# Kernel tuning notes

Hardware: AMD Instinct MI355X
Metric: run time of the kernel (lower is better)

## Reference

```python
import jax, jax.numpy as jnp
import numpy as np

B, TE, TD = 16, 400, 64
E, H = 256, 512
H2 = 2 * H  # 1024
V = 32000


def setup_inputs():
    key = jax.random.key(0)
    k = jax.random.split(key, 16)
    s = 0.05
    return {
        "encoder_inputs": jax.random.randint(k[0], (B, TE), 0, V),
        "decoder_inputs": jax.random.randint(k[1], (B, TD), 0, V),
        "ext_oov_sizes": jax.random.randint(k[2], (B,), 0, 10),
        "enc_idxes_on_ext_voc": jax.random.randint(k[3], (B, TE), 0, V),
        "h0": jnp.zeros((2, B, H), jnp.float32),
        "c0": jnp.zeros((2, B, H), jnp.float32),
        "emb": jax.random.normal(k[4], (V, E)) * 0.1,
        "Wih_f": jax.random.normal(k[5], (4 * H, E)) * s,
        "Whh_f": jax.random.normal(k[6], (4 * H, H)) * s,
        "b_f": jnp.zeros((4 * H,), jnp.float32),
        "Wih_b": jax.random.normal(k[7], (4 * H, E)) * s,
        "Whh_b": jax.random.normal(k[8], (4 * H, H)) * s,
        "b_b": jnp.zeros((4 * H,), jnp.float32),
        "Wih_d": jax.random.normal(k[9], (4 * H2, E + 2 * H2)) * s,
        "Whh_d": jax.random.normal(k[10], (4 * H2, H2)) * s,
        "b_d": jnp.zeros((4 * H2,), jnp.float32),
        "W_ea": jax.random.normal(k[11], (H2, H2)) * 0.006,
        "W_da": jax.random.normal(k[12], (H2, H2)) * 0.006,
        "W_v": jax.random.normal(k[13], (V, 3 * H2)) * s,
        "b_v": jnp.zeros((V,), jnp.float32),
    }


def lstm_cell(x, h, c, Wih, Whh, b):
    z = x @ Wih.T + h @ Whh.T + b
    i, f, g, o = jnp.split(z, 4, axis=-1)
    i, f, o = jax.nn.sigmoid(i), jax.nn.sigmoid(f), jax.nn.sigmoid(o)
    c2 = f * c + i * jnp.tanh(g)
    return o * jnp.tanh(c2), c2


def run_lstm(xs, h0, c0, Wih, Whh, b):
    # xs: [T, B, E]
    def step(carry, x):
        h, c = lstm_cell(x, carry[0], carry[1], Wih, Whh, b)
        return (h, c), h
    (h, c), hs = jax.lax.scan(step, (h0, c0), xs)
    return hs, h, c


def _forward(emb, Wih_f, Whh_f, b_f, Wih_b, Whh_b, b_b, Wih_d, Whh_d, b_d,
             W_ea, W_da, W_v, b_v, h0, c0, encoder_inputs, decoder_inputs):
    xs = emb[encoder_inputs].transpose(1, 0, 2)  # [TE, B, E]
    hs_f, hf, cf = run_lstm(xs, h0[0], c0[0], Wih_f, Whh_f, b_f)
    hs_b, hb, cb = run_lstm(xs[::-1], h0[1], c0[1], Wih_b, Whh_b, b_b)
    enc_out = jnp.concatenate([hs_f, hs_b[::-1]], axis=-1).transpose(1, 0, 2)  # [B, TE, 2H]
    h = jnp.concatenate([hf, hb], axis=-1)  # [B, 2H] (torch reshape of bi-dir last hidden)
    c = jnp.concatenate([cf, cb], axis=-1)
    dec_emb = emb[decoder_inputs].transpose(1, 0, 2)  # [TD, B, E]

    def step(carry, xs_t):
        h, c, accum, buf = carry
        i, emb_t = xs_t
        # intra-temporal encoder attention: exp scores normalized by past accumulation
        scores = jnp.einsum('bd,btd->bt', h @ W_ea, enc_out)  # [B, TE]
        exp_s = jnp.exp(scores)
        denom = jnp.where(i == 0, jnp.ones_like(accum), accum)
        ep = exp_s / denom
        attn = ep / jnp.sum(ep, axis=-1, keepdims=True)
        ctx_e = jnp.einsum('bt,btd->bd', attn, enc_out)
        # intra-decoder attention over previously produced hidden states (masked)
        dsc = jnp.einsum('bd,tbd->bt', h @ W_da, buf)  # [B, TD]
        dsc = jnp.where((jnp.arange(TD) < i)[None, :], dsc, -1e30)
        dw = jnp.where(i == 0, 0.0, jax.nn.softmax(dsc, axis=-1))
        ctx_d = jnp.einsum('bt,tbd->bd', dw, buf)
        x = jnp.concatenate([emb_t, ctx_e, ctx_d], axis=-1)  # [B, E+4H]
        h2, c2 = lstm_cell(x, h, c, Wih_d, Whh_d, b_d)
        buf2 = buf.at[i].set(h2)
        feat = jnp.concatenate([h2, ctx_e, ctx_d], axis=-1)  # [B, 6H]
        logd = jax.nn.log_softmax(feat @ W_v.T + b_v, axis=-1)
        return (h2, c2, accum + exp_s, buf2), logd

    carry0 = (h, c, jnp.zeros((B, TE), h.dtype), jnp.zeros((TD, B, H2), h.dtype))
    (h, c, _, _), logds = jax.lax.scan(step, carry0, (jnp.arange(TD), dec_emb))
    return logds.transpose(1, 0, 2), h[None], c[None]


def reference(encoder_inputs, decoder_inputs, ext_oov_sizes, enc_idxes_on_ext_voc,
              h0, c0, emb, Wih_f, Whh_f, b_f, Wih_b, Whh_b, b_b,
              Wih_d, Whh_d, b_d, W_ea, W_da, W_v, b_v):
    # ext_oov_sizes / enc_idxes_on_ext_voc are unused by forward (as in the torch source)
    return _forward(emb, Wih_f, Whh_f, b_f, Wih_b, Whh_b, b_b, Wih_d, Whh_d, b_d,
                    W_ea, W_da, W_v, b_v, h0, c0, encoder_inputs, decoder_inputs)
```

## Files before the change

### kernel.cpp

```cpp
#include <hip/hip_runtime.h>
#include <math.h>

#define B_  16
#define TE_ 400
#define TD_ 64
#define E_  256
#define H_  512
#define H2_ 1024
#define V_  32000
#define KE_ 768

typedef __attribute__((ext_vector_type(4))) float f32x4;
typedef __attribute__((ext_vector_type(8))) short s16x8;
typedef __attribute__((ext_vector_type(8))) unsigned short u16x8;
typedef __attribute__((ext_vector_type(4))) unsigned short u16x4;

__device__ __forceinline__ float bf2f(unsigned short u){
  union { unsigned int i; float f; } v; v.i = ((unsigned int)u) << 16; return v.f;
}
__device__ __forceinline__ unsigned short f2bf(float f){
  union { float f; unsigned int i; } v; v.f = f;
  return (unsigned short)((v.i + 0x7fffu + ((v.i >> 16) & 1u)) >> 16);
}
__device__ __forceinline__ float sigmoidf_(float x){ return 1.f/(1.f + expf(-x)); }

__device__ __forceinline__ void gl_lds16(const void* gsrc, void* ldst){
  __builtin_amdgcn_global_load_lds(
      (const __attribute__((address_space(1))) unsigned int*)gsrc,
      (__attribute__((address_space(3))) unsigned int*)ldst, 16, 0, 0);
}

__device__ __forceinline__ void bar_arrive(unsigned* obj, unsigned widx){
  __syncthreads();
  if (threadIdx.x == 0){
    __threadfence();
    __hip_atomic_fetch_add(&obj[(widx & 7u)*32], 1u, __ATOMIC_RELAXED, __HIP_MEMORY_SCOPE_AGENT);
  }
}
__device__ __forceinline__ void bar_wait(unsigned* obj, unsigned nwg, unsigned widx, unsigned epoch){
  if (threadIdx.x == 0){
    if (widx == 0){
      for(;;){
        unsigned s = 0;
        #pragma unroll
        for (int k2 = 0; k2 < 8; ++k2)
          s += __hip_atomic_load(&obj[k2*32], __ATOMIC_RELAXED, __HIP_MEMORY_SCOPE_AGENT);
        if (s >= nwg*epoch) break;
      }
      __hip_atomic_store(&obj[256], epoch, __ATOMIC_RELEASE, __HIP_MEMORY_SCOPE_AGENT);
    } else {
      while (__hip_atomic_load(&obj[256], __ATOMIC_RELAXED, __HIP_MEMORY_SCOPE_AGENT) < epoch)
        __builtin_amdgcn_s_sleep(1);
    }
    __threadfence();
  }
  __syncthreads();
}
__device__ __forceinline__ void fast_bar(unsigned* obj, unsigned nwg, unsigned widx, unsigned epoch){
  bar_arrive(obj, widx);
  bar_wait(obj, nwg, widx, epoch);
}

__global__ void k_init(unsigned* bars, float* accum){
  int gid = blockIdx.x*256 + threadIdx.x;
  if (gid < 4096) bars[gid] = 0u;
  if (gid < B_*TE_) accum[gid] = 0.f;
}

__global__ void k_gather(const float* __restrict__ emb, const int* __restrict__ idx,
                         unsigned short* __restrict__ out, int T){
  int wv = threadIdx.x >> 6, l = threadIdx.x & 63;
  int row = blockIdx.x*4 + wv;
  if (row >= T*B_) return;
  int t = row >> 4, b = row & 15;
  int tok = idx[b*T + t];
  float4 v = *(const float4*)(emb + (size_t)tok*E_ + l*4);
  u16x4 o; o[0]=f2bf(v.x); o[1]=f2bf(v.y); o[2]=f2bf(v.z); o[3]=f2bf(v.w);
  *(u16x4*)(out + (size_t)row*E_ + l*4) = o;
}

__global__ void k_prep_enc(const float* __restrict__ Wih_f, const float* __restrict__ Whh_f,
                           const float* __restrict__ Wih_b, const float* __restrict__ Whh_b,
                           unsigned short* __restrict__ Wenc){
  int it = blockIdx.x*256 + threadIdx.x;
  int dir = it / (2048*96); int rem = it % (2048*96);
  int pr = rem / 96; int kc = rem % 96; int k0 = kc*8;
  int g = pr >> 6, r = pr & 63, gate = r >> 4, ul = r & 15;
  int orig = gate*H_ + g*16 + ul;
  const float* Wih = dir ? Wih_b : Wih_f;
  const float* Whh = dir ? Whh_b : Whh_f;
  u16x8 o;
  #pragma unroll
  for (int e = 0; e < 8; ++e){
    int k = k0 + e;
    float v = (k < E_) ? Wih[(size_t)orig*E_ + k] : Whh[(size_t)orig*H_ + (k - E_)];
    o[e] = f2bf(v);
  }
  *(u16x8*)(Wenc + ((size_t)dir*2048 + pr)*KE_ + k0) = o;
}

__global__ void k_prep_whext(const float* __restrict__ Whh_d, const float* __restrict__ W_da,
                             char* __restrict__ WhExt){
  int it = blockIdx.x*256 + threadIdx.x;
  if (it < 524288){
    int g = it >> 13; int rem = it & 8191;
    int kblk = rem >> 10; int rem2 = rem & 1023;
    int row = rem2 >> 4; int k8 = rem2 & 15;
    int gate = row >> 4, ul = row & 15;
    int orig = gate*H2_ + g*16 + ul;
    u16x8 o;
    #pragma unroll
    for (int e = 0; e < 8; ++e)
      o[e] = f2bf(Whh_d[(size_t)orig*H2_ + kblk*128 + k8*8 + e]);
    size_t off = (size_t)g*163840 + (size_t)kblk*20480 + (size_t)(row*256 + ((k8*16) ^ ((row&7)<<4)));
    *(u16x8*)(WhExt + off) = o;
  } else if (it < 655360){
    int qi = it - 524288;
    int g = qi >> 11; int rem = qi & 2047;
    int kblk = rem >> 8; int c2 = rem & 255;
    int wv = c2 >> 6, rr = (c2 >> 2) & 15, c = c2 & 3;
    u16x8 o;
    #pragma unroll
    for (int e = 0; e < 8; ++e)
      o[e] = f2bf(W_da[(size_t)(g*16 + rr)*H2_ + kblk*128 + wv*32 + c*8 + e]);
    size_t off = (size_t)g*163840 + (size_t)kblk*20480 + 16384 + (size_t)(wv*1024 + rr*64 + ((c*16) ^ ((rr&7)<<4)));
    *(u16x8*)(WhExt + off) = o;
  }
}

__global__ void k_prep_ctx(const float* __restrict__ Wih_d, char* __restrict__ CtxW){
  int it = blockIdx.x*256 + threadIdx.x;
  int g = it >> 14; int rem = it & 16383;
  int kblk = rem >> 10; int rem2 = rem & 1023;
  int row = rem2 >> 4; int k8 = rem2 & 15;
  int gate = row >> 4, ul = row & 15;
  int orig = gate*H2_ + g*16 + ul;
  int k = 256 + kblk*128 + k8*8;
  u16x8 o;
  #pragma unroll
  for (int e = 0; e < 8; ++e)
    o[e] = f2bf(Wih_d[(size_t)orig*2304 + k + e]);
  size_t off = (size_t)g*262144 + (size_t)kblk*16384 + (size_t)(row*256 + ((k8*16) ^ ((row&7)<<4)));
  *(u16x8*)(CtxW + off) = o;
}

__global__ void k_prep_wihemb(const float* __restrict__ Wih_d, unsigned short* __restrict__ Wemb){
  int it = blockIdx.x*256 + threadIdx.x;
  int p = it >> 5; int k0 = (it & 31)*8;
  int g = p >> 6, gate = (p >> 4) & 3, ul = p & 15;
  int orig = gate*H2_ + g*16 + ul;
  u16x8 o;
  #pragma unroll
  for (int e = 0; e < 8; ++e)
    o[e] = f2bf(Wih_d[(size_t)orig*2304 + k0 + e]);
  *(u16x8*)(Wemb + (size_t)p*256 + k0) = o;
}

__global__ void __launch_bounds__(256, 2) k_zinit(
    const unsigned short* __restrict__ A,
    const unsigned short* __restrict__ Bw,
    const float* __restrict__ bd,
    float* __restrict__ Cz)
{
  __shared__ unsigned short Ab[128*72];
  __shared__ unsigned short Bt[128*72];
  int p = blockIdx.x;
  int mt = p >> 5, nt = p & 31;
  int m0 = mt*128, n0 = nt*128;
  int tid = threadIdx.x, wvv = tid>>6, l = tid&63;
  int wr = wvv>>1, wc = wvv&1;
  f32x4 zero4 = {0.f,0.f,0.f,0.f};
  f32x4 acc[4][4];
  #pragma unroll
  for (int a=0;a<4;++a){
    #pragma unroll
    for (int b=0;b<4;++b) acc[a][b] = zero4;
  }
  for (int k0 = 0; k0 < 256; k0 += 64){
    #pragma unroll
    for (int qq = 0; qq < 4; ++qq){
      int idx8 = (tid + qq*256)*8;
      int r = idx8 >> 6, k = idx8 & 63;
      *(u16x8*)(Ab + r*72 + k) = *(const u16x8*)(A + (size_t)(m0+r)*256 + k0 + k);
      *(u16x8*)(Bt + r*72 + k) = *(const u16x8*)(Bw + (size_t)(n0+r)*256 + k0 + k);
    }
    __syncthreads();
    #pragma unroll
    for (int ks = 0; ks < 2; ++ks){
      s16x8 af[4], bf[4];
      #pragma unroll
      for (int fi=0;fi<4;++fi)
        af[fi] = *(const s16x8*)(Ab + (wr*64+fi*16+(l&15))*72 + ks*32 + (l>>4)*8);
      #pragma unroll
      for (int fj=0;fj<4;++fj)
        bf[fj] = *(const s16x8*)(Bt + (wc*64+fj*16+(l&15))*72 + ks*32 + (l>>4)*8);
      #pragma unroll
      for (int fi=0;fi<4;++fi){
        #pragma unroll
        for (int fj=0;fj<4;++fj)
          acc[fi][fj] = __builtin_amdgcn_mfma_f32_16x16x32_bf16(af[fi], bf[fj], acc[fi][fj], 0,0,0);
      }
    }
    __syncthreads();
  }
  #pragma unroll
  for (int fj=0;fj<4;++fj){
    int col = n0 + wc*64 + fj*16 + (l&15);
    int orig = ((col>>4)&3)*H2_ + (col>>6)*16 + (col&15);
    float bias = bd[orig];
    #pragma unroll
    for (int fi=0;fi<4;++fi){
      #pragma unroll
      for (int j=0;j<4;++j){
        int row = m0 + wr*64 + fi*16 + (l>>4)*4 + j;
        Cz[(size_t)row*4096 + col] = acc[fi][fj][j] + bias;
      }
    }
  }
}

__global__ void __launch_bounds__(256, 1) k_encoder(
    const unsigned short* __restrict__ xs,
    const unsigned short* __restrict__ Wenc,
    const float* __restrict__ b_f, const float* __restrict__ b_b,
    const float* __restrict__ h0, const float* __restrict__ c0,
    unsigned short* __restrict__ enc_out,
    unsigned short* __restrict__ hbuf,
    float* __restrict__ h0dec, float* __restrict__ c0dec,
    unsigned* __restrict__ bars)
{
  extern __shared__ char smem[];
  unsigned short* Wt = (unsigned short*)smem;
  unsigned short* At = Wt + 64*776;
  float* zl = (float*)(At + 16*776);
  int tid = threadIdx.x;
  int w = blockIdx.x;
  int dir = w >> 5, g = w & 31;
  int wv = tid >> 6, l = tid & 63;
  unsigned* bobj = bars + dir*512;
  {
    const unsigned short* Wsrc = Wenc + ((size_t)dir*2048 + g*64)*KE_;
    int r = tid >> 2, s = tid & 3;
    for (int c = 0; c < 24; ++c)
      *(u16x8*)(Wt + r*776 + s*192 + c*8) = *(const u16x8*)(Wsrc + (size_t)r*KE_ + s*192 + c*8);
  }
  const float* bias = dir ? b_b : b_f;
  int bb = tid >> 4, ul = tid & 15;
  float creg = c0[((size_t)dir*16 + bb)*H_ + g*16 + ul];
  int kchunk = (l >> 4) * 8;
  float bia = bias[wv*H_ + g*16 + (l&15)];
  f32x4 bias4 = { bia, bia, bia, bia };
  f32x4 zero4 = { 0.f, 0.f, 0.f, 0.f };
  {
    int r = tid >> 4, s = tid & 15;
    int tg0 = dir ? (TE_-1) : 0;
    *(u16x8*)(At + r*776 + s*16)     = *(const u16x8*)(xs + ((size_t)tg0*16 + r)*E_ + s*16);
    *(u16x8*)(At + r*776 + s*16 + 8) = *(const u16x8*)(xs + ((size_t)tg0*16 + r)*E_ + s*16 + 8);
    for (int e = 0; e < 32; ++e)
      At[r*776 + 256 + s*32 + e] = f2bf(h0[((size_t)dir*16 + r)*H_ + s*32 + e]);
  }
  __syncthreads();
  for (int t = 0; t < TE_; ++t){
    int tg = dir ? (TE_-1 - t) : t;
    f32x4 acc0 = bias4, acc1 = zero4;
    const unsigned short* brow = Wt + (wv*16 + (l&15))*776 + kchunk;
    const unsigned short* ap   = At + (l&15)*776 + kchunk;
    #pragma unroll
    for (int ks = 0; ks < 24; ++ks){
      s16x8 afr = *(const s16x8*)(ap + ks*32);
      s16x8 bfr = *(const s16x8*)(brow + ks*32);
      if (ks & 1) acc1 = __builtin_amdgcn_mfma_f32_16x16x32_bf16(afr, bfr, acc1, 0, 0, 0);
      else        acc0 = __builtin_amdgcn_mfma_f32_16x16x32_bf16(afr, bfr, acc0, 0, 0, 0);
    }
    f32x4 acc = acc0 + acc1;
    #pragma unroll
    for (int j = 0; j < 4; ++j)
      zl[wv*256 + ((l>>4)*4 + j)*16 + (l&15)] = acc[j];
    __syncthreads();
    float zi = zl[0*256 + bb*16 + ul];
    float zf = zl[1*256 + bb*16 + ul];
    float zg = zl[2*256 + bb*16 + ul];
    float zo = zl[3*256 + bb*16 + ul];
    float iv = sigmoidf_(zi), fv = sigmoidf_(zf), gv = tanhf(zg), ov = sigmoidf_(zo);
    float cc = fv*creg + iv*gv;
    float hh = ov * tanhf(cc);
    creg = cc;
    int u = g*16 + ul;
    unsigned short hb = f2bf(hh);
    hbuf[((size_t)dir*2 + ((t+1)&1))*(16*H_) + bb*H_ + u] = hb;
    enc_out[((size_t)bb*TE_ + tg)*H2_ + dir*H_ + u] = hb;
    if (t == TE_-1){
      h0dec[(size_t)bb*H2_ + dir*H_ + u] = hh;
      c0dec[(size_t)bb*H2_ + dir*H_ + u] = cc;
    }
    bar_arrive(bobj, (unsigned)g);
    if (t+1 < TE_){
      int r = tid >> 4, s = tid & 15;
      int tg2 = dir ? (TE_-2 - t) : (t+1);
      *(u16x8*)(At + r*776 + s*16)     = *(const u16x8*)(xs + ((size_t)tg2*16 + r)*E_ + s*16);
      *(u16x8*)(At + r*776 + s*16 + 8) = *(const u16x8*)(xs + ((size_t)tg2*16 + r)*E_ + s*16 + 8);
    }
    bar_wait(bobj, 32, (unsigned)g, (unsigned)(t+1));
    if (t+1 < TE_){
      int r = tid >> 4, s = tid & 15;
      const unsigned short* hsrc = hbuf + ((size_t)dir*2 + ((t+1)&1))*(16*H_) + r*H_ + s*32;
      for (int c = 0; c < 4; ++c)
        *(u16x8*)(At + r*776 + 256 + s*32 + c*8) = *(const u16x8*)(hsrc + c*8);
    }
    __syncthreads();
  }
}

__global__ void k_dec_init(const float* __restrict__ h0dec, unsigned short* __restrict__ hreg){
  int gid = blockIdx.x*256 + threadIdx.x;
  if (gid < 16384) hreg[gid] = f2bf(h0dec[gid]);
}

__global__ void __launch_bounds__(256, 2) k_penc(
    const unsigned short* __restrict__ enc,
    const float* __restrict__ Wea,
    unsigned short* __restrict__ P)
{
  __shared__ unsigned short Ab[128*72];
  __shared__ unsigned short Bt[128*72];
  int p = blockIdx.x;
  int mt = p >> 3, nt = p & 7;
  int m0 = mt*128, n0 = nt*128;
  int tid = threadIdx.x, wvv = tid>>6, l = tid&63;
  int wr = wvv>>1, wc = wvv&1;
  f32x4 zero4 = {0.f,0.f,0.f,0.f};
  f32x4 acc[4][4];
  #pragma unroll
  for (int a=0;a<4;++a){
    #pragma unroll
    for (int b=0;b<4;++b) acc[a][b] = zero4;
  }
  for (int k0 = 0; k0 < 1024; k0 += 64){
    #pragma unroll
    for (int qq = 0; qq < 4; ++qq){
      int idx8 = (tid + qq*256)*8;
      int r = idx8 >> 6, k = idx8 & 63;
      *(u16x8*)(Ab + r*72 + k) = *(const u16x8*)(enc + (size_t)(m0+r)*1024 + k0 + k);
    }
    #pragma unroll
    for (int qq = 0; qq < 4; ++qq){
      int idx8 = (tid + qq*256)*8;
      int r = idx8 >> 6, k = idx8 & 63;
      const float* src = Wea + (size_t)(n0+r)*1024 + k0 + k;
      float4 v0 = *(const float4*)src;
      float4 v1 = *(const float4*)(src+4);
      u16x8 o;
      o[0]=f2bf(v0.x); o[1]=f2bf(v0.y); o[2]=f2bf(v0.z); o[3]=f2bf(v0.w);
      o[4]=f2bf(v1.x); o[5]=f2bf(v1.y); o[6]=f2bf(v1.z); o[7]=f2bf(v1.w);
      *(u16x8*)(Bt + r*72 + k) = o;
    }
    __syncthreads();
    #pragma unroll
    for (int ks = 0; ks < 2; ++ks){
      s16x8 af[4], bf[4];
      #pragma unroll
      for (int fi=0;fi<4;++fi)
        af[fi] = *(const s16x8*)(Ab + (wr*64+fi*16+(l&15))*72 + ks*32 + (l>>4)*8);
      #pragma unroll
      for (int fj=0;fj<4;++fj)
        bf[fj] = *(const s16x8*)(Bt + (wc*64+fj*16+(l&15))*72 + ks*32 + (l>>4)*8);
      #pragma unroll
      for (int fi=0;fi<4;++fi){
        #pragma unroll
        for (int fj=0;fj<4;++fj)
          acc[fi][fj] = __builtin_amdgcn_mfma_f32_16x16x32_bf16(af[fi], bf[fj], acc[fi][fj], 0,0,0);
      }
    }
    __syncthreads();
  }
  #pragma unroll
  for (int fj=0;fj<4;++fj){
    int col = n0 + wc*64 + fj*16 + (l&15);
    #pragma unroll
    for (int fi=0;fi<4;++fi){
      #pragma unroll
      for (int j=0;j<4;++j){
        int row = m0 + wr*64 + fi*16 + (l>>4)*4 + j;
        P[(size_t)row*1024 + col] = f2bf(acc[fi][fj][j]);
      }
    }
  }
}

__device__ __forceinline__ void issueA(const char* gA, char* Bb, int wv, int l, int kblk, int buf){
  const char* gsrc = gA + (size_t)kblk*20480;
  char* lb = Bb + buf*20480;
  #pragma unroll
  for (int q = 0; q < 4; ++q)
    gl_lds16(gsrc + wv*4096 + q*1024 + (size_t)l*16, lb + wv*4096 + q*1024);
  gl_lds16(gsrc + 16384 + wv*1024 + (size_t)l*16, lb + 16384 + wv*1024);
}
__device__ __forceinline__ void issueC(const char* gC, char* Bb, int wv, int l, int kblk, int buf){
  const char* gsrc = gC + (size_t)kblk*16384;
  char* lb = Bb + buf*20480;
  #pragma unroll
  for (int q = 0; q < 4; ++q)
    gl_lds16(gsrc + wv*4096 + q*1024 + (size_t)l*16, lb + wv*4096 + q*1024);
}

__global__ void __launch_bounds__(256, 1) k_decoder(
  const char* __restrict__ WhExt,
  const char* __restrict__ CtxW,
  const float* __restrict__ zinit,
  const unsigned short* __restrict__ Penc,
  const unsigned short* __restrict__ enc_out,
  const float* __restrict__ c0dec,
  unsigned short* __restrict__ hreg,
  unsigned short* __restrict__ xbuf,
  float* __restrict__ q,
  float* __restrict__ accum,
  float* __restrict__ pctx,
  float* __restrict__ psum,
  unsigned short* __restrict__ bufh,
  unsigned short* __restrict__ Av,
  float* __restrict__ outHC,
  unsigned* __restrict__ bars)
{
  extern __shared__ char smem[];
  int tid = threadIdx.x, w = blockIdx.x;
  int wv = tid >> 6, l = tid & 63;
  unsigned* objA = bars + 1024;
  unsigned* objB = bars + 1536;
  unsigned* objC = bars + 2048;

  unsigned short* Atc = (unsigned short*)smem;
  unsigned short* Ah  = (unsigned short*)smem;
  char*  Bb = smem + 66560;
  float* zl = (float*)(smem + 148480);
  float* zq = (float*)(smem + 152576);
  unsigned short* encL = (unsigned short*)smem;
  float* epL  = (float*)(smem + 102400);
  float* dscL = (float*)(smem + 103424);

  bool isL = (w < 64);
  int eb = 0, ec = 0;
  if (w >= 64){ eb = (w-64) >> 3; ec = (w-64) & 7; }

  if (w >= 64){
    for (int rr = 0; rr < 50; ++rr){
      const unsigned short* src = enc_out + ((size_t)eb*TE_ + ec*50 + rr)*H2_;
      *(u16x4*)(encL + rr*1024 + tid*4) = *(const u16x4*)(src + tid*4);
    }
    __syncthreads();
  }
  float creg = 0.f;
  int bb = tid >> 4, ul = tid & 15;
  const char* gA = (const char*)WhExt + (size_t)w*163840;
  const char* gC = (const char*)CtxW + (size_t)w*262144;

  f32x4 acc0, acc1;

  for (int i = 0; i < TD_; ++i){
    if (isL){
      issueA(gA, Bb, wv, l, 0, 0);
      issueA(gA, Bb, wv, l, 1, 1);
      {
        int r = tid >> 4, s = tid & 15;
        const unsigned short* hsrc = hreg + (i&1)*16384 + r*H2_ + s*64;
        for (int c = 0; c < 8; ++c)
          *(u16x8*)(Ah + r*1032 + s*64 + c*8) = *(const u16x8*)(hsrc + c*8);
      }
      __syncthreads();
      {
        const float* zsrc = zinit + ((size_t)i*16 + (l>>4)*4)*4096 + w*64 + wv*16 + (l&15);
        f32x4 a; a[0]=zsrc[0]; a[1]=zsrc[4096]; a[2]=zsrc[8192]; a[3]=zsrc[12288];
        acc0 = a;
        f32x4 z4 = {0.f,0.f,0.f,0.f};
        acc1 = z4;
      }
      f32x4 accq = {0.f,0.f,0.f,0.f};
      int swz = ((l&7)<<4);
      for (int kblk = 0; kblk < 8; ++kblk){
        int buf = kblk % 3;
        if (kblk + 2 < 8) issueA(gA, Bb, wv, l, kblk+2, (kblk+2)%3);
        if (kblk < 6)       asm volatile("s_waitcnt vmcnt(10)" ::: "memory");
        else if (kblk == 6) asm volatile("s_waitcnt vmcnt(5)" ::: "memory");
        else                asm volatile("s_waitcnt vmcnt(0)" ::: "memory");
        const unsigned short* ap = Ah + (l&15)*1032 + kblk*128 + (l>>4)*8;
        const char* Bz = Bb + buf*20480 + wv*4096;
        #pragma unroll
        for (int ks = 0; ks < 4; ++ks){
          int k8 = ks*4 + (l>>4);
          s16x8 afr = *(const s16x8*)(ap + ks*32);
          s16x8 bfr = *(const s16x8*)(Bz + (l&15)*256 + ((k8*16) ^ swz));
          if (ks & 1) acc1 = __builtin_amdgcn_mfma_f32_16x16x32_bf16(afr, bfr, acc1, 0,0,0);
          else        acc0 = __builtin_amdgcn_mfma_f32_16x16x32_bf16(afr, bfr, acc0, 0,0,0);
        }
        {
          s16x8 afq = *(const s16x8*)(Ah + (l&15)*1032 + kblk*128 + wv*32 + (l>>4)*8);
          s16x8 bfq = *(const s16x8*)(Bb + buf*20480 + 16384 + wv*1024 + (l&15)*64 + ((((l>>4)*16)) ^ swz));
          accq = __builtin_amdgcn_mfma_f32_16x16x32_bf16(afq, bfq, accq, 0,0,0);
        }
      }
      #pragma unroll
      for (int j = 0; j < 4; ++j)
        zq[wv*256 + ((l>>4)*4+j)*16 + (l&15)] = accq[j];
      __syncthreads();
      float qv = zq[0*256 + bb*16 + ul] + zq[1*256 + bb*16 + ul]
               + zq[2*256 + bb*16 + ul] + zq[3*256 + bb*16 + ul];
      q[(size_t)bb*H2_ + w*16 + ul] = qv;
    } else {
      const unsigned short* hb_ = hreg + (i&1)*16384 + eb*H2_ + l*16;
      u16x8 hv0 = *(const u16x8*)hb_;
      u16x8 hv1 = *(const u16x8*)(hb_ + 8);
      float hf[16];
      #pragma unroll
      for (int c = 0; c < 8; ++c){ hf[c] = bf2f(hv0[c]); hf[8+c] = bf2f(hv1[c]); }
      for (int rr = wv; rr < 50; rr += 4){
        const unsigned short* pr = Penc + ((size_t)(eb*TE_ + ec*50 + rr))*H2_ + l*16;
        u16x8 p0 = *(const u16x8*)pr;
        u16x8 p1 = *(const u16x8*)(pr + 8);
        float sc = 0.f;
        #pragma unroll
        for (int c = 0; c < 8; ++c) sc += hf[c]*bf2f(p0[c]);
        #pragma unroll
        for (int c = 0; c < 8; ++c) sc += hf[8+c]*bf2f(p1[c]);
        #pragma unroll
        for (int o = 1; o < 64; o <<= 1) sc += __shfl_xor(sc, o);
        if (l == 0){
          int t = ec*50 + rr;
          float es = expf(sc);
          float aold = accum[eb*TE_ + t];
          float denom = (i == 0) ? 1.f : aold;
          accum[eb*TE_ + t] = aold + es;
          epL[rr] = es / denom;
        }
      }
      __syncthreads();
      float tot = 0.f;
      for (int rr = 0; rr < 50; ++rr) tot += epL[rr];
      float a0=0.f,a1=0.f,a2=0.f,a3=0.f;
      for (int rr = 0; rr < 50; ++rr){
        float wgt = epL[rr];
        u16x4 ev = *(const u16x4*)(encL + rr*1024 + tid*4);
        a0 += wgt*bf2f(ev[0]); a1 += wgt*bf2f(ev[1]); a2 += wgt*bf2f(ev[2]); a3 += wgt*bf2f(ev[3]);
      }
      int slot = w - 64;
      float4 o4; o4.x=a0; o4.y=a1; o4.z=a2; o4.w=a3;
      *(float4*)(pctx + (size_t)slot*1024 + tid*4) = o4;
      if (tid == 0) psum[slot] = tot;
      __syncthreads();
    }
    fast_bar(objA, 192, (unsigned)w, (unsigned)(i+1));

    if (isL){
      #pragma unroll
      for (int j = 0; j < 4; ++j)
        issueC(gC, Bb, wv, l, j, j);
    } else if (w < 96){
      int b = (w-64) >> 1, half = w & 1;
      int col = half*512 + tid*2;
      if (i == 0){
        *(unsigned*)(xbuf + (size_t)b*2048 + 1024 + col) = 0u;
        *(unsigned*)(Av + ((size_t)b*TD_ + i)*3072 + 2048 + col) = 0u;
      } else {
        const float* qp = q + (size_t)b*H2_ + l*16;
        float4 q0 = *(const float4*)(qp);
        float4 q1 = *(const float4*)(qp+4);
        float4 q2 = *(const float4*)(qp+8);
        float4 q3 = *(const float4*)(qp+12);
        for (int tp = wv; tp < i; tp += 4){
          const unsigned short* br = bufh + ((size_t)tp*16 + b)*H2_ + l*16;
          u16x8 e0 = *(const u16x8*)(br);
          u16x8 e1 = *(const u16x8*)(br + 8);
          float sc = q0.x*bf2f(e0[0]) + q0.y*bf2f(e0[1]) + q0.z*bf2f(e0[2]) + q0.w*bf2f(e0[3])
                   + q1.x*bf2f(e0[4]) + q1.y*bf2f(e0[5]) + q1.z*bf2f(e0[6]) + q1.w*bf2f(e0[7])
                   + q2.x*bf2f(e1[0]) + q2.y*bf2f(e1[1]) + q2.z*bf2f(e1[2]) + q2.w*bf2f(e1[3])
                   + q3.x*bf2f(e1[4]) + q3.y*bf2f(e1[5]) + q3.z*bf2f(e1[6]) + q3.w*bf2f(e1[7]);
          #pragma unroll
          for (int o = 1; o < 64; o <<= 1) sc += __shfl_xor(sc, o);
          if (l == 0) dscL[tp] = sc;
        }
        __syncthreads();
        float scv = (l < i) ? dscL[l] : -1e30f;
        float m = scv;
        #pragma unroll
        for (int o = 1; o < 64; o <<= 1) m = fmaxf(m, __shfl_xor(m, o));
        float e = (l < i) ? expf(scv - m) : 0.f;
        float ssum = e;
        #pragma unroll
        for (int o = 1; o < 64; o <<= 1) ssum += __shfl_xor(ssum, o);
        float wgt = e / ssum;
        float c0_ = 0.f, c1_ = 0.f;
        for (int tp = 0; tp < i; ++tp){
          float wt = __shfl(wgt, tp);
          unsigned hv = *(const unsigned*)(bufh + ((size_t)tp*16 + b)*H2_ + col);
          c0_ += wt*bf2f((unsigned short)hv);
          c1_ += wt*bf2f((unsigned short)(hv>>16));
        }
        unsigned o2 = (unsigned)f2bf(c0_) | ((unsigned)f2bf(c1_) << 16);
        *(unsigned*)(xbuf + (size_t)b*2048 + 1024 + col) = o2;
        *(unsigned*)(Av + ((size_t)b*TD_ + i)*3072 + 2048 + col) = o2;
      }
    } else if (w < 112){
      int b = w - 96;
      float sx=0.f, sy=0.f, sz=0.f, sw=0.f, pst=0.f;
      for (int c = 0; c < 8; ++c){
        float4 v = *(const float4*)(pctx + (size_t)(b*8+c)*1024 + tid*4);
        sx += v.x; sy += v.y; sz += v.z; sw += v.w;
        pst += psum[b*8+c];
      }
      float inv = 1.f/pst;
      u16x4 o; o[0]=f2bf(sx*inv); o[1]=f2bf(sy*inv); o[2]=f2bf(sz*inv); o[3]=f2bf(sw*inv);
      *(u16x4*)(xbuf + (size_t)b*2048 + tid*4) = o;
      *(u16x4*)(Av + ((size_t)b*TD_ + i)*3072 + 1024 + tid*4) = o;
    }
    fast_bar(objB, 192, (unsigned)w, (unsigned)(i+1));

    if (isL){
      {
        int r = tid >> 4, s = tid & 15;
        for (int c = 0; c < 16; ++c)
          *(u16x8*)(Atc + r*2056 + s*128 + c*8) = *(const u16x8*)(xbuf + (size_t)r*2048 + s*128 + c*8);
      }
      __syncthreads();
      int swz = ((l&7)<<4);
      for (int kblk = 0; kblk < 16; ++kblk){
        int buf = kblk & 3;
        if (kblk >= 4 && kblk <= 12) asm volatile("s_waitcnt vmcnt(12)" ::: "memory");
        else if (kblk == 13)         asm volatile("s_waitcnt vmcnt(8)" ::: "memory");
        else if (kblk == 14)         asm volatile("s_waitcnt vmcnt(4)" ::: "memory");
        else if (kblk == 15)         asm volatile("s_waitcnt vmcnt(0)" ::: "memory");
        const unsigned short* ap = Atc + (l&15)*2056 + kblk*128 + (l>>4)*8;
        const char* Bz = Bb + buf*20480 + wv*4096;
        #pragma unroll
        for (int ks = 0; ks < 4; ++ks){
          int k8 = ks*4 + (l>>4);
          s16x8 afr = *(const s16x8*)(ap + ks*32);
          s16x8 bfr = *(const s16x8*)(Bz + (l&15)*256 + ((k8*16) ^ swz));
          if (ks & 1) acc1 = __builtin_amdgcn_mfma_f32_16x16x32_bf16(afr, bfr, acc1, 0,0,0);
          else        acc0 = __builtin_amdgcn_mfma_f32_16x16x32_bf16(afr, bfr, acc0, 0,0,0);
        }
        if (kblk + 4 < 16) issueC(gC, Bb, wv, l, kblk+4, buf);
      }
      f32x4 acc = acc0 + acc1;
      #pragma unroll
      for (int j = 0; j < 4; ++j)
        zl[wv*256 + ((l>>4)*4+j)*16 + (l&15)] = acc[j];
      __syncthreads();
      float zi = zl[0*256 + bb*16 + ul];
      float zf = zl[1*256 + bb*16 + ul];
      float zg = zl[2*256 + bb*16 + ul];
      float zo = zl[3*256 + bb*16 + ul];
      if (i == 0) creg = c0dec[(size_t)bb*H2_ + w*16 + ul];
      float iv = sigmoidf_(zi), fv = sigmoidf_(zf), gv = tanhf(zg), ov = sigmoidf_(zo);
      float cc = fv*creg + iv*gv;
      float hh = ov*tanhf(cc);
      creg = cc;
      int u = w*16 + ul;
      unsigned short hb2 = f2bf(hh);
      hreg[((i+1)&1)*16384 + (size_t)bb*H2_ + u] = hb2;
      Av[((size_t)bb*TD_ + i)*3072 + u] = hb2;
      bufh[((size_t)i*16 + bb)*H2_ + u] = hb2;
      if (i == TD_-1){
        outHC[(size_t)bb*H2_ + u] = hh;
        outHC[16384 + (size_t)bb*H2_ + u] = cc;
      }
    }
    fast_bar(objC, 192, (unsigned)w, (unsigned)(i+1));
  }
}

__global__ void __launch_bounds__(256, 2) k_vocab_gemm(
    const unsigned short* __restrict__ Av,
    const float* __restrict__ Wv,
    const float* __restrict__ bv,
    float* __restrict__ out)
{
  __shared__ unsigned short Ab[128*72];
  __shared__ unsigned short Bt[128*72];
  int p = blockIdx.x;
  int mt = (p>>3)&7, nt = (p&7) + 8*(p>>6);
  if (nt >= 250) return;
  int m0 = mt*128, n0 = nt*128;
  int tid = threadIdx.x, wvv = tid>>6, l = tid&63;
  int wr = wvv>>1, wc = wvv&1;
  f32x4 zero4 = {0.f,0.f,0.f,0.f};
  f32x4 acc[4][4];
  #pragma unroll
  for (int a=0;a<4;++a){
    #pragma unroll
    for (int b=0;b<4;++b) acc[a][b] = zero4;
  }
  for (int k0 = 0; k0 < 3072; k0 += 64){
    #pragma unroll
    for (int qq = 0; qq < 4; ++qq){
      int idx8 = (tid + qq*256)*8;
      int r = idx8 >> 6, k = idx8 & 63;
      *(u16x8*)(Ab + r*72 + k) = *(const u16x8*)(Av + (size_t)(m0+r)*3072 + k0 + k);
    }
    #pragma unroll
    for (int qq = 0; qq < 4; ++qq){
      int idx8 = (tid + qq*256)*8;
      int r = idx8 >> 6, k = idx8 & 63;
      const float* src = Wv + (size_t)(n0+r)*3072 + k0 + k;
      float4 v0 = *(const float4*)src;
      float4 v1 = *(const float4*)(src+4);
      u16x8 o;
      o[0]=f2bf(v0.x); o[1]=f2bf(v0.y); o[2]=f2bf(v0.z); o[3]=f2bf(v0.w);
      o[4]=f2bf(v1.x); o[5]=f2bf(v1.y); o[6]=f2bf(v1.z); o[7]=f2bf(v1.w);
      *(u16x8*)(Bt + r*72 + k) = o;
    }
    __syncthreads();
    #pragma unroll
    for (int ks = 0; ks < 2; ++ks){
      s16x8 af[4], bf[4];
      #pragma unroll
      for (int fi=0;fi<4;++fi)
        af[fi] = *(const s16x8*)(Ab + (wr*64+fi*16+(l&15))*72 + ks*32 + (l>>4)*8);
      #pragma unroll
      for (int fj=0;fj<4;++fj)
        bf[fj] = *(const s16x8*)(Bt + (wc*64+fj*16+(l&15))*72 + ks*32 + (l>>4)*8);
      #pragma unroll
      for (int fi=0;fi<4;++fi){
        #pragma unroll
        for (int fj=0;fj<4;++fj)
          acc[fi][fj] = __builtin_amdgcn_mfma_f32_16x16x32_bf16(af[fi], bf[fj], acc[fi][fj], 0,0,0);
      }
    }
    __syncthreads();
  }
  #pragma unroll
  for (int fj=0;fj<4;++fj){
    int col = n0 + wc*64 + fj*16 + (l&15);
    float bias = bv[col];
    #pragma unroll
    for (int fi=0;fi<4;++fi){
      #pragma unroll
      for (int j=0;j<4;++j){
        int row = m0 + wr*64 + fi*16 + (l>>4)*4 + j;
        out[(size_t)row*V_ + col] = acc[fi][fj][j] + bias;
      }
    }
  }
}

__global__ void k_logsoftmax(float* __restrict__ out){
  int row = blockIdx.x;
  float* x = out + (size_t)row*V_;
  int tid = threadIdx.x;
  __shared__ float red[64];
  float m = -1e30f;
  for (int c = tid; c < V_; c += 256) m = fmaxf(m, x[c]);
  #pragma unroll
  for (int o=1;o<64;o<<=1) m = fmaxf(m, __shfl_xor(m,o));
  if ((tid&63)==0) red[tid>>6] = m;
  __syncthreads();
  m = fmaxf(fmaxf(red[0],red[1]), fmaxf(red[2],red[3]));
  float s = 0.f;
  for (int c = tid; c < V_; c += 256) s += expf(x[c]-m);
  #pragma unroll
  for (int o=1;o<64;o<<=1) s += __shfl_xor(s,o);
  if ((tid&63)==0) red[8 + (tid>>6)] = s;
  __syncthreads();
  s = red[8]+red[9]+red[10]+red[11];
  float lse = m + logf(s);
  for (int c = tid; c < V_; c += 256) x[c] = x[c] - lse;
}

extern "C" void kernel_launch(void* const* d_in, const int* in_sizes, int n_in,
                              void* d_out, int out_size, void* d_ws, size_t ws_size,
                              hipStream_t stream){
  (void)in_sizes; (void)n_in; (void)out_size; (void)ws_size;
  const int*   enc_in = (const int*)d_in[0];
  const int*   dec_in = (const int*)d_in[1];
  const float* h0   = (const float*)d_in[4];
  const float* c0   = (const float*)d_in[5];
  const float* emb  = (const float*)d_in[6];
  const float* Wih_f= (const float*)d_in[7];
  const float* Whh_f= (const float*)d_in[8];
  const float* b_f  = (const float*)d_in[9];
  const float* Wih_b= (const float*)d_in[10];
  const float* Whh_b= (const float*)d_in[11];
  const float* b_b  = (const float*)d_in[12];
  const float* Wih_d= (const float*)d_in[13];
  const float* Whh_d= (const float*)d_in[14];
  const float* b_d  = (const float*)d_in[15];
  const float* W_ea = (const float*)d_in[16];
  const float* W_da = (const float*)d_in[17];
  const float* W_v  = (const float*)d_in[18];
  const float* b_v  = (const float*)d_in[19];
  float* out = (float*)d_out;
  char* ws = (char*)d_ws;

  size_t o_bars   = 0;
  size_t o_accum  = 16384;
  size_t o_q      = o_accum + 25600;
  size_t o_xs     = o_q + 65536;
  size_t o_decemb = o_xs + (size_t)6400*256*2;
  size_t o_Wenc   = o_decemb + (size_t)1024*256*2;
  size_t o_WhExt  = o_Wenc + (size_t)2*2048*768*2;
  size_t o_CtxW   = o_WhExt + (size_t)64*163840;
  size_t o_Wemb   = o_CtxW + (size_t)64*262144;
  size_t o_zinit  = o_Wemb + (size_t)4096*256*2;
  size_t o_enc    = o_zinit + (size_t)1024*4096*4;
  size_t o_Penc   = o_enc + (size_t)16*400*1024*2;
  size_t o_hbuf   = o_Penc + (size_t)16*400*1024*2;
  size_t o_h0dec  = o_hbuf + (size_t)2*2*16*512*2;
  size_t o_c0dec  = o_h0dec + (size_t)16*1024*4;
  size_t o_hreg   = o_c0dec + (size_t)16*1024*4;
  size_t o_xbuf   = o_hreg + (size_t)2*16*1024*2;
  size_t o_pctx   = o_xbuf + (size_t)16*2048*2;
  size_t o_psum   = o_pctx + (size_t)128*1024*4;
  size_t o_bufh   = o_psum + 512;
  size_t o_Av     = o_bufh + (size_t)64*16*1024*2;

  unsigned* bars        = (unsigned*)(ws + o_bars);
  float* accum          = (float*)(ws + o_accum);
  float* q              = (float*)(ws + o_q);
  unsigned short* xs    = (unsigned short*)(ws + o_xs);
  unsigned short* decemb= (unsigned short*)(ws + o_decemb);
  unsigned short* Wenc  = (unsigned short*)(ws + o_Wenc);
  char* WhExt           = ws + o_WhExt;
  char* CtxW            = ws + o_CtxW;
  unsigned short* Wemb  = (unsigned short*)(ws + o_Wemb);
  float* zinit          = (float*)(ws + o_zinit);
  unsigned short* encO  = (unsigned short*)(ws + o_enc);
  unsigned short* Penc  = (unsigned short*)(ws + o_Penc);
  unsigned short* hbuf  = (unsigned short*)(ws + o_hbuf);
  float* h0dec          = (float*)(ws + o_h0dec);
  float* c0dec          = (float*)(ws + o_c0dec);
  unsigned short* hreg  = (unsigned short*)(ws + o_hreg);
  unsigned short* xbuf  = (unsigned short*)(ws + o_xbuf);
  float* pctx           = (float*)(ws + o_pctx);
  float* psum           = (float*)(ws + o_psum);
  unsigned short* bufh  = (unsigned short*)(ws + o_bufh);
  unsigned short* Av    = (unsigned short*)(ws + o_Av);

  hipFuncSetAttribute((const void*)k_encoder, hipFuncAttributeMaxDynamicSharedMemorySize, 131072);
  hipFuncSetAttribute((const void*)k_decoder, hipFuncAttributeMaxDynamicSharedMemorySize, 157696);

  k_init<<<26, 256, 0, stream>>>(bars, accum);
  k_gather<<<1600, 256, 0, stream>>>(emb, enc_in, xs, TE_);
  k_gather<<<256, 256, 0, stream>>>(emb, dec_in, decemb, TD_);
  k_prep_enc<<<1536, 256, 0, stream>>>(Wih_f, Whh_f, Wih_b, Whh_b, Wenc);
  k_prep_whext<<<2560, 256, 0, stream>>>(Whh_d, W_da, WhExt);
  k_prep_ctx<<<4096, 256, 0, stream>>>(Wih_d, CtxW);
  k_prep_wihemb<<<512, 256, 0, stream>>>(Wih_d, Wemb);
  k_zinit<<<256, 256, 0, stream>>>(decemb, Wemb, b_d, zinit);
  k_encoder<<<64, 256, 128512, stream>>>(xs, Wenc, b_f, b_b, h0, c0, encO, hbuf, h0dec, c0dec, bars);
  k_penc<<<400, 256, 0, stream>>>(encO, W_ea, Penc);
  k_dec_init<<<64, 256, 0, stream>>>(h0dec, hreg);
  k_decoder<<<192, 256, 156672, stream>>>(WhExt, CtxW, zinit, Penc, encO, c0dec,
                                          hreg, xbuf, q, accum, pctx, psum, bufh, Av,
                                          out + (size_t)32768000, bars);
  k_vocab_gemm<<<2048, 256, 0, stream>>>(Av, W_v, b_v, out);
  k_logsoftmax<<<1024, 256, 0, stream>>>(out);
}
```

Baseline: 6.342 ms.

## Hoist encoder input projection, overlap weight prep with encoder, restructure decoder sync

A new batched MFMA GEMM computes the encoder input projections (x·Wih + bias) for all timesteps ahead of time, so the recurrent encoder loop only multiplies by Whh (K=512 instead of 768). Decoder weight preparation moves into extra workgroups of the encoder launch so it runs alongside the sequential recurrence. The global barrier is replaced with per-timestep counters and backoff polling. The decoder is reorganised into specialised roles (matrix, encoder attention, decoder attention) that synchronise through separate barriers and accumulate context with atomics. These changes cost extra workspace for the zx buffer, add atomic traffic, and make correctness depend on more complex synchronisation.

```diff
diff --git a/kernel.cpp b/kernel.cpp
--- a/kernel.cpp
+++ b/kernel.cpp
@@ -8,7 +8,6 @@
 #define H_  512
 #define H2_ 1024
 #define V_  32000
-#define KE_ 768
 
 typedef __attribute__((ext_vector_type(4))) float f32x4;
 typedef __attribute__((ext_vector_type(8))) short s16x8;
@@ -30,41 +29,30 @@
       (__attribute__((address_space(3))) unsigned int*)ldst, 16, 0, 0);
 }
 
-__device__ __forceinline__ void bar_arrive(unsigned* obj, unsigned widx){
-  __syncthreads();
-  if (threadIdx.x == 0){
-    __threadfence();
-    __hip_atomic_fetch_add(&obj[(widx & 7u)*32], 1u, __ATOMIC_RELAXED, __HIP_MEMORY_SCOPE_AGENT);
-  }
-}
-__device__ __forceinline__ void bar_wait(unsigned* obj, unsigned nwg, unsigned widx, unsigned epoch){
-  if (threadIdx.x == 0){
-    if (widx == 0){
-      for(;;){
-        unsigned s = 0;
-        #pragma unroll
-        for (int k2 = 0; k2 < 8; ++k2)
-          s += __hip_atomic_load(&obj[k2*32], __ATOMIC_RELAXED, __HIP_MEMORY_SCOPE_AGENT);
-        if (s >= nwg*epoch) break;
-      }
-      __hip_atomic_store(&obj[256], epoch, __ATOMIC_RELEASE, __HIP_MEMORY_SCOPE_AGENT);
-    } else {
-      while (__hip_atomic_load(&obj[256], __ATOMIC_RELAXED, __HIP_MEMORY_SCOPE_AGENT) < epoch)
-        __builtin_amdgcn_s_sleep(1);
-    }
-    __threadfence();
-  }
-  __syncthreads();
-}
-__device__ __forceinline__ void fast_bar(unsigned* obj, unsigned nwg, unsigned widx, unsigned epoch){
-  bar_arrive(obj, widx);
-  bar_wait(obj, nwg, widx, epoch);
-}
-
-__global__ void k_init(unsigned* bars, float* accum){
+__device__ __forceinline__ void arrive8(unsigned* inst){
+  __threadfence();
+  __hip_atomic_fetch_add(inst + (blockIdx.x & 7u)*16, 1u, __ATOMIC_RELAXED, __HIP_MEMORY_SCOPE_AGENT);
+}
+__device__ __forceinline__ void poll8(unsigned* inst, unsigned target){
+  int it = 0;
+  for(;;){
+    unsigned s = 0;
+    #pragma unroll
+    for (int k = 0; k < 8; ++k)
+      s += __hip_atomic_load(inst + k*16, __ATOMIC_RELAXED, __HIP_MEMORY_SCOPE_AGENT);
+    if (s >= target) break;
+    if (it < 6) __builtin_amdgcn_s_sleep(1);
+    else if (it < 24) __builtin_amdgcn_s_sleep(4);
+    else __builtin_amdgcn_s_sleep(16);
+    ++it;
+  }
+}
+
+__global__ void k_init(unsigned* bars, float* ctxn, float* psumT){
   int gid = blockIdx.x*256 + threadIdx.x;
-  if (gid < 4096) bars[gid] = 0u;
-  if (gid < B_*TE_) accum[gid] = 0.f;
+  if (gid < 81920) bars[gid] = 0u;
+  if (gid < 32768) ctxn[gid] = 0.f;
+  if (gid < 32) psumT[gid] = 0.f;
 }
 
 __global__ void k_gather(const float* __restrict__ emb, const int* __restrict__ idx,
@@ -96,12 +84,12 @@
     float v = (k < E_) ? Wih[(size_t)orig*E_ + k] : Whh[(size_t)orig*H_ + (k - E_)];
     o[e] = f2bf(v);
   }
-  *(u16x8*)(Wenc + ((size_t)dir*2048 + pr)*KE_ + k0) = o;
-}
-
-__global__ void k_prep_whext(const float* __restrict__ Whh_d, const float* __restrict__ W_da,
-                             char* __restrict__ WhExt){
-  int it = blockIdx.x*256 + threadIdx.x;
+  *(u16x8*)(Wenc + ((size_t)dir*2048 + pr)*768 + k0) = o;
+}
+
+__device__ __forceinline__ void prep_whext_item(int it, const float* __restrict__ Whh_d,
+                                                const float* __restrict__ W_da,
+                                                char* __restrict__ WhExt){
   if (it < 524288){
     int g = it >> 13; int rem = it & 8191;
     int kblk = rem >> 10; int rem2 = rem & 1023;
@@ -118,18 +106,20 @@
     int qi = it - 524288;
     int g = qi >> 11; int rem = qi & 2047;
     int kblk = rem >> 8; int c2 = rem & 255;
-    int wv = c2 >> 6, rr = (c2 >> 2) & 15, c = c2 & 3;
+    int wvv = c2 >> 6, rr = (c2 >> 2) & 15, c = c2 & 3;
+    int row = g*16 + rr;
     u16x8 o;
     #pragma unroll
     for (int e = 0; e < 8; ++e)
-      o[e] = f2bf(W_da[(size_t)(g*16 + rr)*H2_ + kblk*128 + wv*32 + c*8 + e]);
-    size_t off = (size_t)g*163840 + (size_t)kblk*20480 + 16384 + (size_t)(wv*1024 + rr*64 + ((c*16) ^ ((rr&7)<<4)));
+      o[e] = f2bf(W_da[(size_t)row*H2_ + kblk*128 + wvv*32 + c*8 + e]);
+    size_t off = (size_t)g*163840 + (size_t)kblk*20480 + 16384
+               + (size_t)(wvv*1024 + rr*64 + ((c*16) ^ ((rr&3)<<4)));
     *(u16x8*)(WhExt + off) = o;
   }
 }
 
-__global__ void k_prep_ctx(const float* __restrict__ Wih_d, char* __restrict__ CtxW){
-  int it = blockIdx.x*256 + threadIdx.x;
+__device__ __forceinline__ void prep_ctx_item(int it, const float* __restrict__ Wih_d,
+                                              char* __restrict__ CtxW){
   int g = it >> 14; int rem = it & 16383;
   int kblk = rem >> 10; int rem2 = rem & 1023;
   int row = rem2 >> 4; int k8 = rem2 & 15;
@@ -219,54 +209,194 @@
   }
 }
 
-__global__ void __launch_bounds__(256, 1) k_encoder(
+__global__ void __launch_bounds__(256, 2) k_zx(
     const unsigned short* __restrict__ xs,
     const unsigned short* __restrict__ Wenc,
     const float* __restrict__ b_f, const float* __restrict__ b_b,
+    unsigned short* __restrict__ zx)
+{
+  __shared__ unsigned short Ab[128*72];
+  __shared__ unsigned short Bt[128*72];
+  int pblk = blockIdx.x;
+  int dir = pblk / 800; int rem = pblk % 800;
+  int mt = rem >> 4, nt = rem & 15;
+  int m0 = mt*128, n0 = nt*128;
+  int tid = threadIdx.x, wvv = tid>>6, l = tid&63;
+  int wr = wvv>>1, wc = wvv&1;
+  f32x4 zero4 = {0.f,0.f,0.f,0.f};
+  f32x4 acc[4][4];
+  #pragma unroll
+  for (int a=0;a<4;++a){
+    #pragma unroll
+    for (int b=0;b<4;++b) acc[a][b] = zero4;
+  }
+  for (int k0 = 0; k0 < 256; k0 += 64){
+    #pragma unroll
+    for (int qq = 0; qq < 4; ++qq){
+      int idx8 = (tid + qq*256)*8;
+      int r = idx8 >> 6, k = idx8 & 63;
+      *(u16x8*)(Ab + r*72 + k) = *(const u16x8*)(xs + (size_t)(m0+r)*256 + k0 + k);
+      *(u16x8*)(Bt + r*72 + k) = *(const u16x8*)(Wenc + ((size_t)dir*2048 + n0+r)*768 + k0 + k);
+    }
+    __syncthreads();
+    #pragma unroll
+    for (int ks = 0; ks < 2; ++ks){
+      s16x8 af[4], bf[4];
+      #pragma unroll
+      for (int fi=0;fi<4;++fi)
+        af[fi] = *(const s16x8*)(Ab + (wr*64+fi*16+(l&15))*72 + ks*32 + (l>>4)*8);
+      #pragma unroll
+      for (int fj=0;fj<4;++fj)
+        bf[fj] = *(const s16x8*)(Bt + (wc*64+fj*16+(l&15))*72 + ks*32 + (l>>4)*8);
+      #pragma unroll
+      for (int fi=0;fi<4;++fi){
+        #pragma unroll
+        for (int fj=0;fj<4;++fj)
+          acc[fi][fj] = __builtin_amdgcn_mfma_f32_16x16x32_bf16(af[fi], bf[fj], acc[fi][fj], 0,0,0);
+      }
+    }
+    __syncthreads();
+  }
+  const float* bsrc = dir ? b_b : b_f;
+  #pragma unroll
+  for (int fj=0;fj<4;++fj){
+    int col = n0 + wc*64 + fj*16 + (l&15);
+    float bias = bsrc[((col>>4)&3)*512 + (col>>6)*16 + (col&15)];
+    #pragma unroll
+    for (int fi=0;fi<4;++fi){
+      #pragma unroll
+      for (int j=0;j<4;++j){
+        int row = m0 + wr*64 + fi*16 + (l>>4)*4 + j;
+        zx[((size_t)dir*6400 + row)*2048 + col] = f2bf(acc[fi][fj][j] + bias);
+      }
+    }
+  }
+}
+
+__global__ void __launch_bounds__(256, 2) k_penc(
+    const unsigned short* __restrict__ enc,
+    const float* __restrict__ Wea,
+    unsigned short* __restrict__ P)
+{
+  __shared__ unsigned short Ab[128*72];
+  __shared__ unsigned short Bt[128*72];
+  int p = blockIdx.x;
+  int mt = p >> 3, nt = p & 7;
+  int m0 = mt*128, n0 = nt*128;
+  int tid = threadIdx.x, wvv = tid>>6, l = tid&63;
+  int wr = wvv>>1, wc = wvv&1;
+  f32x4 zero4 = {0.f,0.f,0.f,0.f};
+  f32x4 acc[4][4];
+  #pragma unroll
+  for (int a=0;a<4;++a){
+    #pragma unroll
+    for (int b=0;b<4;++b) acc[a][b] = zero4;
+  }
+  for (int k0 = 0; k0 < 1024; k0 += 64){
+    #pragma unroll
+    for (int qq = 0; qq < 4; ++qq){
+      int idx8 = (tid + qq*256)*8;
+      int r = idx8 >> 6, k = idx8 & 63;
+      *(u16x8*)(Ab + r*72 + k) = *(const u16x8*)(enc + (size_t)(m0+r)*1024 + k0 + k);
+    }
+    #pragma unroll
+    for (int qq = 0; qq < 4; ++qq){
+      int idx8 = (tid + qq*256)*8;
+      int r = idx8 >> 6, k = idx8 & 63;
+      const float* src = Wea + (size_t)(n0+r)*1024 + k0 + k;
+      float4 v0 = *(const float4*)src;
+      float4 v1 = *(const float4*)(src+4);
+      u16x8 o;
+      o[0]=f2bf(v0.x); o[1]=f2bf(v0.y); o[2]=f2bf(v0.z); o[3]=f2bf(v0.w);
+      o[4]=f2bf(v1.x); o[5]=f2bf(v1.y); o[6]=f2bf(v1.z); o[7]=f2bf(v1.w);
+      *(u16x8*)(Bt + r*72 + k) = o;
+    }
+    __syncthreads();
+    #pragma unroll
+    for (int ks = 0; ks < 2; ++ks){
+      s16x8 af[4], bf[4];
+      #pragma unroll
+      for (int fi=0;fi<4;++fi)
+        af[fi] = *(const s16x8*)(Ab + (wr*64+fi*16+(l&15))*72 + ks*32 + (l>>4)*8);
+      #pragma unroll
+      for (int fj=0;fj<4;++fj)
+        bf[fj] = *(const s16x8*)(Bt + (wc*64+fj*16+(l&15))*72 + ks*32 + (l>>4)*8);
+      #pragma unroll
+      for (int fi=0;fi<4;++fi){
+        #pragma unroll
+        for (int fj=0;fj<4;++fj)
+          acc[fi][fj] = __builtin_amdgcn_mfma_f32_16x16x32_bf16(af[fi], bf[fj], acc[fi][fj], 0,0,0);
+      }
+    }
+    __syncthreads();
+  }
+  #pragma unroll
+  for (int fj=0;fj<4;++fj){
+    int col = n0 + wc*64 + fj*16 + (l&15);
+    #pragma unroll
+    for (int fi=0;fi<4;++fi){
+      #pragma unroll
+      for (int j=0;j<4;++j){
+        int row = m0 + wr*64 + fi*16 + (l>>4)*4 + j;
+        P[(size_t)row*1024 + col] = f2bf(acc[fi][fj][j]);
+      }
+    }
+  }
+}
+
+__global__ void __launch_bounds__(256, 1) k_encoder(
+    const unsigned short* __restrict__ zx,
+    const unsigned short* __restrict__ Wenc,
     const float* __restrict__ h0, const float* __restrict__ c0,
     unsigned short* __restrict__ enc_out,
     unsigned short* __restrict__ hbuf,
     float* __restrict__ h0dec, float* __restrict__ c0dec,
-    unsigned* __restrict__ bars)
+    unsigned* __restrict__ bars,
+    const float* __restrict__ Whh_d, const float* __restrict__ W_da,
+    const float* __restrict__ Wih_d,
+    char* __restrict__ WhExt, char* __restrict__ CtxW)
 {
   extern __shared__ char smem[];
-  unsigned short* Wt = (unsigned short*)smem;
-  unsigned short* At = Wt + 64*776;
-  float* zl = (float*)(At + 16*776);
   int tid = threadIdx.x;
   int w = blockIdx.x;
+  if (w >= 64){
+    int base = (w - 64)*256 + tid;
+    for (int it = base; it < 655360; it += 36864) prep_whext_item(it, Whh_d, W_da, WhExt);
+    for (int it = base; it < 1048576; it += 36864) prep_ctx_item(it, Wih_d, CtxW);
+    return;
+  }
+  unsigned short* Wt = (unsigned short*)smem;
+  unsigned short* At = Wt + 64*520;
+  float* zl = (float*)(At + 16*520);
   int dir = w >> 5, g = w & 31;
   int wv = tid >> 6, l = tid & 63;
-  unsigned* bobj = bars + dir*512;
   {
-    const unsigned short* Wsrc = Wenc + ((size_t)dir*2048 + g*64)*KE_;
+    const unsigned short* Wsrc = Wenc + ((size_t)dir*2048 + g*64)*768 + 256;
     int r = tid >> 2, s = tid & 3;
-    for (int c = 0; c < 24; ++c)
-      *(u16x8*)(Wt + r*776 + s*192 + c*8) = *(const u16x8*)(Wsrc + (size_t)r*KE_ + s*192 + c*8);
-  }
-  const float* bias = dir ? b_b : b_f;
+    for (int c = 0; c < 16; ++c)
+      *(u16x8*)(Wt + r*520 + s*128 + c*8) = *(const u16x8*)(Wsrc + (size_t)r*768 + s*128 + c*8);
+  }
   int bb = tid >> 4, ul = tid & 15;
   float creg = c0[((size_t)dir*16 + bb)*H_ + g*16 + ul];
   int kchunk = (l >> 4) * 8;
-  float bia = bias[wv*H_ + g*16 + (l&15)];
-  f32x4 bias4 = { bia, bia, bia, bia };
   f32x4 zero4 = { 0.f, 0.f, 0.f, 0.f };
   {
     int r = tid >> 4, s = tid & 15;
-    int tg0 = dir ? (TE_-1) : 0;
-    *(u16x8*)(At + r*776 + s*16)     = *(const u16x8*)(xs + ((size_t)tg0*16 + r)*E_ + s*16);
-    *(u16x8*)(At + r*776 + s*16 + 8) = *(const u16x8*)(xs + ((size_t)tg0*16 + r)*E_ + s*16 + 8);
     for (int e = 0; e < 32; ++e)
-      At[r*776 + 256 + s*32 + e] = f2bf(h0[((size_t)dir*16 + r)*H_ + s*32 + e]);
-  }
+      At[r*520 + s*32 + e] = f2bf(h0[((size_t)dir*16 + r)*H_ + s*32 + e]);
+  }
+  int tg0 = dir ? (TE_-1) : 0;
+  const unsigned short* zrow = zx + ((size_t)dir*6400 + (size_t)tg0*16 + (l>>4)*4)*2048 + g*64 + wv*16 + (l&15);
+  f32x4 a0cur;
+  a0cur[0]=bf2f(zrow[0]); a0cur[1]=bf2f(zrow[2048]); a0cur[2]=bf2f(zrow[4096]); a0cur[3]=bf2f(zrow[6144]);
   __syncthreads();
   for (int t = 0; t < TE_; ++t){
     int tg = dir ? (TE_-1 - t) : t;
-    f32x4 acc0 = bias4, acc1 = zero4;
-    const unsigned short* brow = Wt + (wv*16 + (l&15))*776 + kchunk;
-    const unsigned short* ap   = At + (l&15)*776 + kchunk;
-    #pragma unroll
-    for (int ks = 0; ks < 24; ++ks){
+    f32x4 acc0 = a0cur, acc1 = zero4;
+    const unsigned short* brow = Wt + (wv*16 + (l&15))*520 + kchunk;
+    const unsigned short* ap   = At + (l&15)*520 + kchunk;
+    #pragma unroll
+    for (int ks = 0; ks < 16; ++ks){
       s16x8 afr = *(const s16x8*)(ap + ks*32);
       s16x8 bfr = *(const s16x8*)(brow + ks*32);
       if (ks & 1) acc1 = __builtin_amdgcn_mfma_f32_16x16x32_bf16(afr, bfr, acc1, 0, 0, 0);
@@ -293,19 +423,37 @@
       h0dec[(size_t)bb*H2_ + dir*H_ + u] = hh;
       c0dec[(size_t)bb*H2_ + dir*H_ + u] = cc;
     }
-    bar_arrive(bobj, (unsigned)g);
+    unsigned* cnt = bars + (size_t)(dir*400 + t)*64;
+    __syncthreads();
+    if (tid == 0){
+      __threadfence();
+      __hip_atomic_fetch_add(cnt + (g&3)*16, 1u, __ATOMIC_RELAXED, __HIP_MEMORY_SCOPE_AGENT);
+    }
     if (t+1 < TE_){
-      int r = tid >> 4, s = tid & 15;
       int tg2 = dir ? (TE_-2 - t) : (t+1);
-      *(u16x8*)(At + r*776 + s*16)     = *(const u16x8*)(xs + ((size_t)tg2*16 + r)*E_ + s*16);
-      *(u16x8*)(At + r*776 + s*16 + 8) = *(const u16x8*)(xs + ((size_t)tg2*16 + r)*E_ + s*16 + 8);
-    }
-    bar_wait(bobj, 32, (unsigned)g, (unsigned)(t+1));
+      const unsigned short* zr2 = zx + ((size_t)dir*6400 + (size_t)tg2*16 + (l>>4)*4)*2048 + g*64 + wv*16 + (l&15);
+      a0cur[0]=bf2f(zr2[0]); a0cur[1]=bf2f(zr2[2048]); a0cur[2]=bf2f(zr2[4096]); a0cur[3]=bf2f(zr2[6144]);
+    }
+    if (tid == 0){
+      int it = 0;
+      for(;;){
+        unsigned s_ = 0;
+        #pragma unroll
+        for (int k2 = 0; k2 < 4; ++k2)
+          s_ += __hip_atomic_load(cnt + k2*16, __ATOMIC_RELAXED, __HIP_MEMORY_SCOPE_AGENT);
+        if (s_ >= 32) break;
+        if (it < 6) __builtin_amdgcn_s_sleep(1);
+        else __builtin_amdgcn_s_sleep(4);
+        ++it;
+      }
+      __threadfence();
+    }
+    __syncthreads();
     if (t+1 < TE_){
       int r = tid >> 4, s = tid & 15;
       const unsigned short* hsrc = hbuf + ((size_t)dir*2 + ((t+1)&1))*(16*H_) + r*H_ + s*32;
       for (int c = 0; c < 4; ++c)
-        *(u16x8*)(At + r*776 + 256 + s*32 + c*8) = *(const u16x8*)(hsrc + c*8);
+        *(u16x8*)(At + r*520 + s*32 + c*8) = *(const u16x8*)(hsrc + c*8);
     }
     __syncthreads();
   }
@@ -316,88 +464,17 @@
   if (gid < 16384) hreg[gid] = f2bf(h0dec[gid]);
 }
 
-__global__ void __launch_bounds__(256, 2) k_penc(
-    const unsigned short* __restrict__ enc,
-    const float* __restrict__ Wea,
-    unsigned short* __restrict__ P)
-{
-  __shared__ unsigned short Ab[128*72];
-  __shared__ unsigned short Bt[128*72];
-  int p = blockIdx.x;
-  int mt = p >> 3, nt = p & 7;
-  int m0 = mt*128, n0 = nt*128;
-  int tid = threadIdx.x, wvv = tid>>6, l = tid&63;
-  int wr = wvv>>1, wc = wvv&1;
-  f32x4 zero4 = {0.f,0.f,0.f,0.f};
-  f32x4 acc[4][4];
-  #pragma unroll
-  for (int a=0;a<4;++a){
-    #pragma unroll
-    for (int b=0;b<4;++b) acc[a][b] = zero4;
-  }
-  for (int k0 = 0; k0 < 1024; k0 += 64){
-    #pragma unroll
-    for (int qq = 0; qq < 4; ++qq){
-      int idx8 = (tid + qq*256)*8;
-      int r = idx8 >> 6, k = idx8 & 63;
-      *(u16x8*)(Ab + r*72 + k) = *(const u16x8*)(enc + (size_t)(m0+r)*1024 + k0 + k);
-    }
-    #pragma unroll
-    for (int qq = 0; qq < 4; ++qq){
-      int idx8 = (tid + qq*256)*8;
-      int r = idx8 >> 6, k = idx8 & 63;
-      const float* src = Wea + (size_t)(n0+r)*1024 + k0 + k;
-      float4 v0 = *(const float4*)src;
-      float4 v1 = *(const float4*)(src+4);
-      u16x8 o;
-      o[0]=f2bf(v0.x); o[1]=f2bf(v0.y); o[2]=f2bf(v0.z); o[3]=f2bf(v0.w);
-      o[4]=f2bf(v1.x); o[5]=f2bf(v1.y); o[6]=f2bf(v1.z); o[7]=f2bf(v1.w);
-      *(u16x8*)(Bt + r*72 + k) = o;
-    }
-    __syncthreads();
-    #pragma unroll
-    for (int ks = 0; ks < 2; ++ks){
-      s16x8 af[4], bf[4];
-      #pragma unroll
-      for (int fi=0;fi<4;++fi)
-        af[fi] = *(const s16x8*)(Ab + (wr*64+fi*16+(l&15))*72 + ks*32 + (l>>4)*8);
-      #pragma unroll
-      for (int fj=0;fj<4;++fj)
-        bf[fj] = *(const s16x8*)(Bt + (wc*64+fj*16+(l&15))*72 + ks*32 + (l>>4)*8);
-      #pragma unroll
-      for (int fi=0;fi<4;++fi){
-        #pragma unroll
-        for (int fj=0;fj<4;++fj)
-          acc[fi][fj] = __builtin_amdgcn_mfma_f32_16x16x32_bf16(af[fi], bf[fj], acc[fi][fj], 0,0,0);
-      }
-    }
-    __syncthreads();
-  }
-  #pragma unroll
-  for (int fj=0;fj<4;++fj){
-    int col = n0 + wc*64 + fj*16 + (l&15);
-    #pragma unroll
-    for (int fi=0;fi<4;++fi){
-      #pragma unroll
-      for (int j=0;j<4;++j){
-        int row = m0 + wr*64 + fi*16 + (l>>4)*4 + j;
-        P[(size_t)row*1024 + col] = f2bf(acc[fi][fj][j]);
-      }
-    }
-  }
-}
-
-__device__ __forceinline__ void issueA(const char* gA, char* Bb, int wv, int l, int kblk, int buf){
+__device__ __forceinline__ void issueA(const char* gA, char* BbA, int wv, int l, int kblk, int buf){
   const char* gsrc = gA + (size_t)kblk*20480;
-  char* lb = Bb + buf*20480;
+  char* lb = BbA + buf*20480;
   #pragma unroll
   for (int q = 0; q < 4; ++q)
     gl_lds16(gsrc + wv*4096 + q*1024 + (size_t)l*16, lb + wv*4096 + q*1024);
   gl_lds16(gsrc + 16384 + wv*1024 + (size_t)l*16, lb + 16384 + wv*1024);
 }
-__device__ __forceinline__ void issueC(const char* gC, char* Bb, int wv, int l, int kblk, int buf){
+__device__ __forceinline__ void issueC(const char* gC, char* BbC, int wv, int l, int kblk, int buf){
   const char* gsrc = gC + (size_t)kblk*16384;
-  char* lb = Bb + buf*20480;
+  char* lb = BbC + buf*16384;
   #pragma unroll
   for (int q = 0; q < 4; ++q)
     gl_lds16(gsrc + wv*4096 + q*1024 + (size_t)l*16, lb + wv*4096 + q*1024);
@@ -412,10 +489,9 @@
   const float* __restrict__ c0dec,
   unsigned short* __restrict__ hreg,
   unsigned short* __restrict__ xbuf,
-  float* __restrict__ q,
-  float* __restrict__ accum,
-  float* __restrict__ pctx,
-  float* __restrict__ psum,
+  float* __restrict__ ctxn,
+  float* __restrict__ psumT,
+  unsigned short* __restrict__ vbuf,
   unsigned short* __restrict__ bufh,
   unsigned short* __restrict__ Av,
   float* __restrict__ outHC,
@@ -424,65 +500,72 @@
   extern __shared__ char smem[];
   int tid = threadIdx.x, w = blockIdx.x;
   int wv = tid >> 6, l = tid & 63;
-  unsigned* objA = bars + 1024;
-  unsigned* objB = bars + 1536;
-  unsigned* objC = bars + 2048;
+  unsigned* dbase = bars + 51200;
 
   unsigned short* Atc = (unsigned short*)smem;
   unsigned short* Ah  = (unsigned short*)smem;
-  char*  Bb = smem + 66560;
-  float* zl = (float*)(smem + 148480);
-  float* zq = (float*)(smem + 152576);
+  char* BbA = smem + 66560;
+  char* BbC = smem + 128000;
+  float* zq = (float*)(smem + 66560);
+  float* zl = (float*)(smem + 128000);
   unsigned short* encL = (unsigned short*)smem;
-  float* epL  = (float*)(smem + 102400);
-  float* dscL = (float*)(smem + 103424);
-
-  bool isL = (w < 64);
+  float* epL  = (float*)(smem + 103424);
+  float* accL = (float*)(smem + 103680);
+  float* dscL = (float*)smem;
+
+  bool isZ = (w < 64);
+  bool isE = (w >= 64 && w < 192);
   int eb = 0, ec = 0;
-  if (w >= 64){ eb = (w-64) >> 3; ec = (w-64) & 7; }
-
-  if (w >= 64){
+  if (isE){ eb = (w-64) >> 3; ec = (w-64) & 7; }
+  int db = w - 192;
+
+  if (isE){
     for (int rr = 0; rr < 50; ++rr){
       const unsigned short* src = enc_out + ((size_t)eb*TE_ + ec*50 + rr)*H2_;
-      *(u16x4*)(encL + rr*1024 + tid*4) = *(const u16x4*)(src + tid*4);
-    }
+      *(u16x4*)(encL + rr*1032 + tid*4) = *(const u16x4*)(src + tid*4);
+    }
+    if (tid < 50) accL[tid] = 0.f;
     __syncthreads();
   }
   float creg = 0.f;
   int bb = tid >> 4, ul = tid & 15;
-  const char* gA = (const char*)WhExt + (size_t)w*163840;
-  const char* gC = (const char*)CtxW + (size_t)w*262144;
-
+  const char* gA = WhExt + (size_t)w*163840;
+  const char* gC = CtxW + (size_t)w*262144;
   f32x4 acc0, acc1;
 
   for (int i = 0; i < TD_; ++i){
-    if (isL){
-      issueA(gA, Bb, wv, l, 0, 0);
-      issueA(gA, Bb, wv, l, 1, 1);
+    int p = i & 1;
+    unsigned* barM = dbase + (size_t)(i*3+0)*128;
+    unsigned* barA = dbase + (size_t)(i*3+1)*128;
+    unsigned* barB = dbase + (size_t)(i*3+2)*128;
+
+    if (isZ){
+      ctxn[(p^1)*16384 + w*256 + tid] = 0.f;
+      if (w == 0 && tid < 16) psumT[(p^1)*16 + tid] = 0.f;
+      const float* zsrc = zinit + ((size_t)i*16 + (l>>4)*4)*4096 + w*64 + wv*16 + (l&15);
+      f32x4 a0i; a0i[0]=zsrc[0]; a0i[1]=zsrc[4096]; a0i[2]=zsrc[8192]; a0i[3]=zsrc[12288];
+      issueA(gA, BbA, wv, l, 0, 0);
+      issueA(gA, BbA, wv, l, 1, 1);
       {
         int r = tid >> 4, s = tid & 15;
-        const unsigned short* hsrc = hreg + (i&1)*16384 + r*H2_ + s*64;
+        const unsigned short* hsrc = hreg + p*16384 + r*H2_ + s*64;
         for (int c = 0; c < 8; ++c)
           *(u16x8*)(Ah + r*1032 + s*64 + c*8) = *(const u16x8*)(hsrc + c*8);
       }
       __syncthreads();
-      {
-        const float* zsrc = zinit + ((size_t)i*16 + (l>>4)*4)*4096 + w*64 + wv*16 + (l&15);
-        f32x4 a; a[0]=zsrc[0]; a[1]=zsrc[4096]; a[2]=zsrc[8192]; a[3]=zsrc[12288];
-        acc0 = a;
-        f32x4 z4 = {0.f,0.f,0.f,0.f};
-        acc1 = z4;
-      }
-      f32x4 accq = {0.f,0.f,0.f,0.f};
+      acc0 = a0i;
+      f32x4 z4 = {0.f,0.f,0.f,0.f};
+      acc1 = z4;
+      f32x4 accv = z4;
       int swz = ((l&7)<<4);
       for (int kblk = 0; kblk < 8; ++kblk){
         int buf = kblk % 3;
-        if (kblk + 2 < 8) issueA(gA, Bb, wv, l, kblk+2, (kblk+2)%3);
+        if (kblk + 2 < 8) issueA(gA, BbA, wv, l, kblk+2, (kblk+2)%3);
         if (kblk < 6)       asm volatile("s_waitcnt vmcnt(10)" ::: "memory");
         else if (kblk == 6) asm volatile("s_waitcnt vmcnt(5)" ::: "memory");
         else                asm volatile("s_waitcnt vmcnt(0)" ::: "memory");
         const unsigned short* ap = Ah + (l&15)*1032 + kblk*128 + (l>>4)*8;
-        const char* Bz = Bb + buf*20480 + wv*4096;
+        const char* Bz = BbA + buf*20480 + wv*4096;
         #pragma unroll
         for (int ks = 0; ks < 4; ++ks){
           int k8 = ks*4 + (l>>4);
@@ -491,143 +574,51 @@
           if (ks & 1) acc1 = __builtin_amdgcn_mfma_f32_16x16x32_bf16(afr, bfr, acc1, 0,0,0);
           else        acc0 = __builtin_amdgcn_mfma_f32_16x16x32_bf16(afr, bfr, acc0, 0,0,0);
         }
-        {
-          s16x8 afq = *(const s16x8*)(Ah + (l&15)*1032 + kblk*128 + wv*32 + (l>>4)*8);
-          s16x8 bfq = *(const s16x8*)(Bb + buf*20480 + 16384 + wv*1024 + (l&15)*64 + ((((l>>4)*16)) ^ swz));
-          accq = __builtin_amdgcn_mfma_f32_16x16x32_bf16(afq, bfq, accq, 0,0,0);
-        }
-      }
+        s16x8 afq = *(const s16x8*)(Ah + (l&15)*1032 + kblk*128 + wv*32 + (l>>4)*8);
+        s16x8 bfv = *(const s16x8*)(BbA + buf*20480 + 16384 + wv*1024 + (l&15)*64 + ((((l>>4)*16)) ^ ((l&3)<<4)));
+        accv = __builtin_amdgcn_mfma_f32_16x16x32_bf16(afq, bfv, accv, 0,0,0);
+      }
+      __syncthreads();
       #pragma unroll
       for (int j = 0; j < 4; ++j)
-        zq[wv*256 + ((l>>4)*4+j)*16 + (l&15)] = accq[j];
-      __syncthreads();
-      float qv = zq[0*256 + bb*16 + ul] + zq[1*256 + bb*16 + ul]
-               + zq[2*256 + bb*16 + ul] + zq[3*256 + bb*16 + ul];
-      q[(size_t)bb*H2_ + w*16 + ul] = qv;
-    } else {
-      const unsigned short* hb_ = hreg + (i&1)*16384 + eb*H2_ + l*16;
-      u16x8 hv0 = *(const u16x8*)hb_;
-      u16x8 hv1 = *(const u16x8*)(hb_ + 8);
-      float hf[16];
-      #pragma unroll
-      for (int c = 0; c < 8; ++c){ hf[c] = bf2f(hv0[c]); hf[8+c] = bf2f(hv1[c]); }
-      for (int rr = wv; rr < 50; rr += 4){
-        const unsigned short* pr = Penc + ((size_t)(eb*TE_ + ec*50 + rr))*H2_ + l*16;
-        u16x8 p0 = *(const u16x8*)pr;
-        u16x8 p1 = *(const u16x8*)(pr + 8);
-        float sc = 0.f;
-        #pragma unroll
-        for (int c = 0; c < 8; ++c) sc += hf[c]*bf2f(p0[c]);
-        #pragma unroll
-        for (int c = 0; c < 8; ++c) sc += hf[8+c]*bf2f(p1[c]);
-        #pragma unroll
-        for (int o = 1; o < 64; o <<= 1) sc += __shfl_xor(sc, o);
-        if (l == 0){
-          int t = ec*50 + rr;
-          float es = expf(sc);
-          float aold = accum[eb*TE_ + t];
-          float denom = (i == 0) ? 1.f : aold;
-          accum[eb*TE_ + t] = aold + es;
-          epL[rr] = es / denom;
-        }
-      }
-      __syncthreads();
-      float tot = 0.f;
-      for (int rr = 0; rr < 50; ++rr) tot += epL[rr];
-      float a0=0.f,a1=0.f,a2=0.f,a3=0.f;
-      for (int rr = 0; rr < 50; ++rr){
-        float wgt = epL[rr];
-        u16x4 ev = *(const u16x4*)(encL + rr*1024 + tid*4);
-        a0 += wgt*bf2f(ev[0]); a1 += wgt*bf2f(ev[1]); a2 += wgt*bf2f(ev[2]); a3 += wgt*bf2f(ev[3]);
-      }
-      int slot = w - 64;
-      float4 o4; o4.x=a0; o4.y=a1; o4.z=a2; o4.w=a3;
-      *(float4*)(pctx + (size_t)slot*1024 + tid*4) = o4;
-      if (tid == 0) psum[slot] = tot;
-      __syncthreads();
-    }
-    fast_bar(objA, 192, (unsigned)w, (unsigned)(i+1));
-
-    if (isL){
-      #pragma unroll
-      for (int j = 0; j < 4; ++j)
-        issueC(gC, Bb, wv, l, j, j);
-    } else if (w < 96){
-      int b = (w-64) >> 1, half = w & 1;
-      int col = half*512 + tid*2;
-      if (i == 0){
-        *(unsigned*)(xbuf + (size_t)b*2048 + 1024 + col) = 0u;
-        *(unsigned*)(Av + ((size_t)b*TD_ + i)*3072 + 2048 + col) = 0u;
-      } else {
-        const float* qp = q + (size_t)b*H2_ + l*16;
-        float4 q0 = *(const float4*)(qp);
-        float4 q1 = *(const float4*)(qp+4);
-        float4 q2 = *(const float4*)(qp+8);
-        float4 q3 = *(const float4*)(qp+12);
-        for (int tp = wv; tp < i; tp += 4){
-          const unsigned short* br = bufh + ((size_t)tp*16 + b)*H2_ + l*16;
-          u16x8 e0 = *(const u16x8*)(br);
-          u16x8 e1 = *(const u16x8*)(br + 8);
-          float sc = q0.x*bf2f(e0[0]) + q0.y*bf2f(e0[1]) + q0.z*bf2f(e0[2]) + q0.w*bf2f(e0[3])
-                   + q1.x*bf2f(e0[4]) + q1.y*bf2f(e0[5]) + q1.z*bf2f(e0[6]) + q1.w*bf2f(e0[7])
-                   + q2.x*bf2f(e1[0]) + q2.y*bf2f(e1[1]) + q2.z*bf2f(e1[2]) + q2.w*bf2f(e1[3])
-                   + q3.x*bf2f(e1[4]) + q3.y*bf2f(e1[5]) + q3.z*bf2f(e1[6]) + q3.w*bf2f(e1[7]);
-          #pragma unroll
-          for (int o = 1; o < 64; o <<= 1) sc += __shfl_xor(sc, o);
-          if (l == 0) dscL[tp] = sc;
-        }
-        __syncthreads();
-        float scv = (l < i) ? dscL[l] : -1e30f;
-        float m = scv;
-        #pragma unroll
-        for (int o = 1; o < 64; o <<= 1) m = fmaxf(m, __shfl_xor(m, o));
-        float e = (l < i) ? expf(scv - m) : 0.f;
-        float ssum = e;
-        #pragma unroll
-        for (int o = 1; o < 64; o <<= 1) ssum += __shfl_xor(ssum, o);
-        float wgt = e / ssum;
-        float c0_ = 0.f, c1_ = 0.f;
-        for (int tp = 0; tp < i; ++tp){
-          float wt = __shfl(wgt, tp);
-          unsigned hv = *(const unsigned*)(bufh + ((size_t)tp*16 + b)*H2_ + col);
-          c0_ += wt*bf2f((unsigned short)hv);
-          c1_ += wt*bf2f((unsigned short)(hv>>16));
-        }
-        unsigned o2 = (unsigned)f2bf(c0_) | ((unsigned)f2bf(c1_) << 16);
-        *(unsigned*)(xbuf + (size_t)b*2048 + 1024 + col) = o2;
-        *(unsigned*)(Av + ((size_t)b*TD_ + i)*3072 + 2048 + col) = o2;
-      }
-    } else if (w < 112){
-      int b = w - 96;
-      float sx=0.f, sy=0.f, sz=0.f, sw=0.f, pst=0.f;
-      for (int c = 0; c < 8; ++c){
-        float4 v = *(const float4*)(pctx + (size_t)(b*8+c)*1024 + tid*4);
-        sx += v.x; sy += v.y; sz += v.z; sw += v.w;
-        pst += psum[b*8+c];
-      }
-      float inv = 1.f/pst;
-      u16x4 o; o[0]=f2bf(sx*inv); o[1]=f2bf(sy*inv); o[2]=f2bf(sz*inv); o[3]=f2bf(sw*inv);
-      *(u16x4*)(xbuf + (size_t)b*2048 + tid*4) = o;
-      *(u16x4*)(Av + ((size_t)b*TD_ + i)*3072 + 1024 + tid*4) = o;
-    }
-    fast_bar(objB, 192, (unsigned)w, (unsigned)(i+1));
-
-    if (isL){
+        zq[wv*256 + ((l>>4)*4+j)*16 + (l&15)] = accv[j];
+      __syncthreads();
+      if (i > 0){
+        float vv = zq[0*256+bb*16+ul] + zq[1*256+bb*16+ul] + zq[2*256+bb*16+ul] + zq[3*256+bb*16+ul];
+        vbuf[((size_t)(i-1)*16 + bb)*H2_ + w*16 + ul] = f2bf(vv);
+      }
+      __syncthreads();
+      if (tid == 0) arrive8(barM);
+      issueC(gC, BbC, wv, l, 0, 0);
+      issueC(gC, BbC, wv, l, 1, 1);
+      if (tid == 0){ poll8(barA, 144); __threadfence(); }
+      __syncthreads();
       {
         int r = tid >> 4, s = tid & 15;
-        for (int c = 0; c < 16; ++c)
-          *(u16x8*)(Atc + r*2056 + s*128 + c*8) = *(const u16x8*)(xbuf + (size_t)r*2048 + s*128 + c*8);
-      }
-      __syncthreads();
-      int swz = ((l&7)<<4);
-      for (int kblk = 0; kblk < 16; ++kblk){
-        int buf = kblk & 3;
-        if (kblk >= 4 && kblk <= 12) asm volatile("s_waitcnt vmcnt(12)" ::: "memory");
-        else if (kblk == 13)         asm volatile("s_waitcnt vmcnt(8)" ::: "memory");
-        else if (kblk == 14)         asm volatile("s_waitcnt vmcnt(4)" ::: "memory");
-        else if (kblk == 15)         asm volatile("s_waitcnt vmcnt(0)" ::: "memory");
-        const unsigned short* ap = Atc + (l&15)*2056 + kblk*128 + (l>>4)*8;
-        const char* Bz = Bb + buf*20480 + wv*4096;
+        float inv = 1.f / psumT[p*16 + r];
+        const float* cn = ctxn + p*16384 + (size_t)r*1024 + s*64;
+        for (int c8 = 0; c8 < 8; ++c8){
+          float4 v0 = *(const float4*)(cn + c8*8);
+          float4 v1 = *(const float4*)(cn + c8*8 + 4);
+          u16x8 o;
+          o[0]=f2bf(v0.x*inv); o[1]=f2bf(v0.y*inv); o[2]=f2bf(v0.z*inv); o[3]=f2bf(v0.w*inv);
+          o[4]=f2bf(v1.x*inv); o[5]=f2bf(v1.y*inv); o[6]=f2bf(v1.z*inv); o[7]=f2bf(v1.w*inv);
+          *(u16x8*)(Atc + r*2056 + s*64 + c8*8) = o;
+        }
+        const unsigned short* xd = xbuf + (size_t)r*1024 + s*64;
+        for (int c8 = 0; c8 < 8; ++c8)
+          *(u16x8*)(Atc + r*2056 + 1024 + s*64 + c8*8) = *(const u16x8*)(xd + c8*8);
+      }
+      {
+        float val = ctxn[p*16384 + (size_t)bb*1024 + w*16 + ul] / psumT[p*16 + bb];
+        Av[((size_t)bb*TD_ + i)*3072 + 1024 + w*16 + ul] = f2bf(val);
+      }
+      __syncthreads();
+      for (int k = 0; k < 16; ++k){
+        if (k < 15) asm volatile("s_waitcnt vmcnt(4)" ::: "memory");
+        else        asm volatile("s_waitcnt vmcnt(0)" ::: "memory");
+        const unsigned short* ap = Atc + (l&15)*2056 + k*128 + (l>>4)*8;
+        const char* Bz = BbC + (k&1)*16384 + wv*4096;
         #pragma unroll
         for (int ks = 0; ks < 4; ++ks){
           int k8 = ks*4 + (l>>4);
@@ -636,8 +627,9 @@
           if (ks & 1) acc1 = __builtin_amdgcn_mfma_f32_16x16x32_bf16(afr, bfr, acc1, 0,0,0);
           else        acc0 = __builtin_amdgcn_mfma_f32_16x16x32_bf16(afr, bfr, acc0, 0,0,0);
         }
-        if (kblk + 4 < 16) issueC(gC, Bb, wv, l, kblk+4, buf);
-      }
+        if (k + 2 < 16) issueC(gC, BbC, wv, l, k+2, k&1);
+      }
+      __syncthreads();
       f32x4 acc = acc0 + acc1;
       #pragma unroll
       for (int j = 0; j < 4; ++j)
@@ -661,8 +653,102 @@
         outHC[(size_t)bb*H2_ + u] = hh;
         outHC[16384 + (size_t)bb*H2_ + u] = cc;
       }
-    }
-    fast_bar(objC, 192, (unsigned)w, (unsigned)(i+1));
+      __syncthreads();
+      if (tid == 0){ arrive8(barB); poll8(barB, 64); __threadfence(); }
+      __syncthreads();
+    } else if (isE){
+      const unsigned short* hb_ = hreg + p*16384 + eb*H2_ + l*16;
+      u16x8 hv0 = *(const u16x8*)hb_;
+      u16x8 hv1 = *(const u16x8*)(hb_ + 8);
+      float hf[16];
+      #pragma unroll
+      for (int c = 0; c < 8; ++c){ hf[c] = bf2f(hv0[c]); hf[8+c] = bf2f(hv1[c]); }
+      for (int rr = wv; rr < 50; rr += 4){
+        const unsigned short* pr = Penc + ((size_t)(eb*TE_ + ec*50 + rr))*H2_ + l*16;
+        u16x8 p0 = *(const u16x8*)pr;
+        u16x8 p1 = *(const u16x8*)(pr + 8);
+        float sc = 0.f;
+        #pragma unroll
+        for (int c = 0; c < 8; ++c) sc += hf[c]*bf2f(p0[c]);
+        #pragma unroll
+        for (int c = 0; c < 8; ++c) sc += hf[8+c]*bf2f(p1[c]);
+        #pragma unroll
+        for (int o = 1; o < 64; o <<= 1) sc += __shfl_xor(sc, o);
+        if (l == 0){
+          float es = expf(sc);
+          float aold = accL[rr];
+          float denom = (i == 0) ? 1.f : aold;
+          accL[rr] = aold + es;
+          epL[rr] = es / denom;
+        }
+      }
+      __syncthreads();
+      float tot = 0.f;
+      for (int rr = 0; rr < 50; ++rr) tot += epL[rr];
+      float a0=0.f,a1=0.f,a2=0.f,a3=0.f;
+      for (int rr = 0; rr < 50; ++rr){
+        float wgt = epL[rr];
+        u16x4 ev = *(const u16x4*)(encL + rr*1032 + tid*4);
+        a0 += wgt*bf2f(ev[0]); a1 += wgt*bf2f(ev[1]); a2 += wgt*bf2f(ev[2]); a3 += wgt*bf2f(ev[3]);
+      }
+      float* dst = ctxn + p*16384 + (size_t)eb*1024 + tid*4;
+      atomicAdd(dst+0, a0); atomicAdd(dst+1, a1); atomicAdd(dst+2, a2); atomicAdd(dst+3, a3);
+      if (tid == 0) atomicAdd(psumT + p*16 + eb, tot);
+      __syncthreads();
+      if (tid == 0){ arrive8(barA); poll8(barB, 64); __threadfence(); }
+      __syncthreads();
+    } else {
+      int col = tid*4;
+      if (i == 0){
+        u16x4 z4v = {0,0,0,0};
+        *(u16x4*)(xbuf + (size_t)db*1024 + col) = z4v;
+        *(u16x4*)(Av + ((size_t)db*TD_ + i)*3072 + 2048 + col) = z4v;
+      } else {
+        if (tid == 0){ poll8(barM, 64); __threadfence(); }
+        __syncthreads();
+        const unsigned short* hq = hreg + p*16384 + db*H2_ + l*16;
+        u16x8 h0v = *(const u16x8*)hq;
+        u16x8 h1v = *(const u16x8*)(hq + 8);
+        float qf[16];
+        #pragma unroll
+        for (int c = 0; c < 8; ++c){ qf[c] = bf2f(h0v[c]); qf[8+c] = bf2f(h1v[c]); }
+        for (int tp = wv; tp < i; tp += 4){
+          const unsigned short* vr = vbuf + ((size_t)tp*16 + db)*H2_ + l*16;
+          u16x8 e0 = *(const u16x8*)vr;
+          u16x8 e1 = *(const u16x8*)(vr + 8);
+          float sc = 0.f;
+          #pragma unroll
+          for (int c = 0; c < 8; ++c) sc += qf[c]*bf2f(e0[c]);
+          #pragma unroll
+          for (int c = 0; c < 8; ++c) sc += qf[8+c]*bf2f(e1[c]);
+          #pragma unroll
+          for (int o = 1; o < 64; o <<= 1) sc += __shfl_xor(sc, o);
+          if (l == 0) dscL[tp] = sc;
+        }
+        __syncthreads();
+        float scv = (l < i) ? dscL[l] : -1e30f;
+        float m = scv;
+        #pragma unroll
+        for (int o = 1; o < 64; o <<= 1) m = fmaxf(m, __shfl_xor(m, o));
+        float e = (l < i) ? expf(scv - m) : 0.f;
+        float ssum = e;
+        #pragma unroll
+        for (int o = 1; o < 64; o <<= 1) ssum += __shfl_xor(ssum, o);
+        float wgt = e / ssum;
+        float c0_=0.f,c1_=0.f,c2_=0.f,c3_=0.f;
+        for (int tp = 0; tp < i; ++tp){
+          float wt = __shfl(wgt, tp);
+          u16x4 hv = *(const u16x4*)(bufh + ((size_t)tp*16 + db)*H2_ + col);
+          c0_ += wt*bf2f(hv[0]); c1_ += wt*bf2f(hv[1]); c2_ += wt*bf2f(hv[2]); c3_ += wt*bf2f(hv[3]);
+        }
+        u16x4 o4; o4[0]=f2bf(c0_); o4[1]=f2bf(c1_); o4[2]=f2bf(c2_); o4[3]=f2bf(c3_);
+        *(u16x4*)(xbuf + (size_t)db*1024 + col) = o4;
+        *(u16x4*)(Av + ((size_t)db*TD_ + i)*3072 + 2048 + col) = o4;
+      }
+      __syncthreads();
+      if (tid == 0){ arrive8(barA); poll8(barB, 64); __threadfence(); }
+      __syncthreads();
+    }
   }
 }
 
@@ -789,30 +875,30 @@
   char* ws = (char*)d_ws;
 
   size_t o_bars   = 0;
-  size_t o_accum  = 16384;
-  size_t o_q      = o_accum + 25600;
-  size_t o_xs     = o_q + 65536;
+  size_t o_ctxn   = 327680;
+  size_t o_psumT  = o_ctxn + 131072;
+  size_t o_xs     = o_psumT + 256;
   size_t o_decemb = o_xs + (size_t)6400*256*2;
   size_t o_Wenc   = o_decemb + (size_t)1024*256*2;
   size_t o_WhExt  = o_Wenc + (size_t)2*2048*768*2;
   size_t o_CtxW   = o_WhExt + (size_t)64*163840;
   size_t o_Wemb   = o_CtxW + (size_t)64*262144;
   size_t o_zinit  = o_Wemb + (size_t)4096*256*2;
-  size_t o_enc    = o_zinit + (size_t)1024*4096*4;
+  size_t o_zx     = o_zinit + (size_t)1024*4096*4;
+  size_t o_enc    = o_zx + (size_t)2*6400*2048*2;
   size_t o_Penc   = o_enc + (size_t)16*400*1024*2;
   size_t o_hbuf   = o_Penc + (size_t)16*400*1024*2;
   size_t o_h0dec  = o_hbuf + (size_t)2*2*16*512*2;
   size_t o_c0dec  = o_h0dec + (size_t)16*1024*4;
   size_t o_hreg   = o_c0dec + (size_t)16*1024*4;
   size_t o_xbuf   = o_hreg + (size_t)2*16*1024*2;
-  size_t o_pctx   = o_xbuf + (size_t)16*2048*2;
-  size_t o_psum   = o_pctx + (size_t)128*1024*4;
-  size_t o_bufh   = o_psum + 512;
+  size_t o_vbuf   = o_xbuf + (size_t)16*1024*2;
+  size_t o_bufh   = o_vbuf + (size_t)64*16*1024*2;
   size_t o_Av     = o_bufh + (size_t)64*16*1024*2;
 
   unsigned* bars        = (unsigned*)(ws + o_bars);
-  float* accum          = (float*)(ws + o_accum);
-  float* q              = (float*)(ws + o_q);
+  float* ctxn           = (float*)(ws + o_ctxn);
+  float* psumT          = (float*)(ws + o_psumT);
   unsigned short* xs    = (unsigned short*)(ws + o_xs);
   unsigned short* decemb= (unsigned short*)(ws + o_decemb);
   unsigned short* Wenc  = (unsigned short*)(ws + o_Wenc);
@@ -820,6 +906,7 @@
   char* CtxW            = ws + o_CtxW;
   unsigned short* Wemb  = (unsigned short*)(ws + o_Wemb);
   float* zinit          = (float*)(ws + o_zinit);
+  unsigned short* zx    = (unsigned short*)(ws + o_zx);
   unsigned short* encO  = (unsigned short*)(ws + o_enc);
   unsigned short* Penc  = (unsigned short*)(ws + o_Penc);
   unsigned short* hbuf  = (unsigned short*)(ws + o_hbuf);
@@ -827,27 +914,26 @@
   float* c0dec          = (float*)(ws + o_c0dec);
   unsigned short* hreg  = (unsigned short*)(ws + o_hreg);
   unsigned short* xbuf  = (unsigned short*)(ws + o_xbuf);
-  float* pctx           = (float*)(ws + o_pctx);
-  float* psum           = (float*)(ws + o_psum);
+  unsigned short* vbuf  = (unsigned short*)(ws + o_vbuf);
   unsigned short* bufh  = (unsigned short*)(ws + o_bufh);
   unsigned short* Av    = (unsigned short*)(ws + o_Av);
 
-  hipFuncSetAttribute((const void*)k_encoder, hipFuncAttributeMaxDynamicSharedMemorySize, 131072);
-  hipFuncSetAttribute((const void*)k_decoder, hipFuncAttributeMaxDynamicSharedMemorySize, 157696);
-
-  k_init<<<26, 256, 0, stream>>>(bars, accum);
+  hipFuncSetAttribute((const void*)k_encoder, hipFuncAttributeMaxDynamicSharedMemorySize, 90000);
+  hipFuncSetAttribute((const void*)k_decoder, hipFuncAttributeMaxDynamicSharedMemorySize, 160768);
+
+  k_init<<<320, 256, 0, stream>>>(bars, ctxn, psumT);
   k_gather<<<1600, 256, 0, stream>>>(emb, enc_in, xs, TE_);
   k_gather<<<256, 256, 0, stream>>>(emb, dec_in, decemb, TD_);
   k_prep_enc<<<1536, 256, 0, stream>>>(Wih_f, Whh_f, Wih_b, Whh_b, Wenc);
-  k_prep_whext<<<2560, 256, 0, stream>>>(Whh_d, W_da, WhExt);
-  k_prep_ctx<<<4096, 256, 0, stream>>>(Wih_d, CtxW);
   k_prep_wihemb<<<512, 256, 0, stream>>>(Wih_d, Wemb);
   k_zinit<<<256, 256, 0, stream>>>(decemb, Wemb, b_d, zinit);
-  k_encoder<<<64, 256, 128512, stream>>>(xs, Wenc, b_f, b_b, h0, c0, encO, hbuf, h0dec, c0dec, bars);
+  k_zx<<<1600, 256, 0, stream>>>(xs, Wenc, b_f, b_b, zx);
+  k_encoder<<<208, 256, 87296, stream>>>(zx, Wenc, h0, c0, encO, hbuf, h0dec, c0dec, bars,
+                                         Whh_d, W_da, Wih_d, WhExt, CtxW);
   k_penc<<<400, 256, 0, stream>>>(encO, W_ea, Penc);
   k_dec_init<<<64, 256, 0, stream>>>(h0dec, hreg);
-  k_decoder<<<192, 256, 156672, stream>>>(WhExt, CtxW, zinit, Penc, encO, c0dec,
-                                          hreg, xbuf, q, accum, pctx, psum, bufh, Av,
+  k_decoder<<<208, 256, 160768, stream>>>(WhExt, CtxW, zinit, Penc, encO, c0dec,
+                                          hreg, xbuf, ctxn, psumT, vbuf, bufh, Av,
                                           out + (size_t)32768000, bars);
   k_vocab_gemm<<<2048, 256, 0, stream>>>(Av, W_v, b_v, out);
   k_logsoftmax<<<1024, 256, 0, stream>>>(out);
```

After: 5.538 ms. 12.7% less time.
